# Performance work log

Measured on AMD Instinct MI355X. Metric: run time of the kernel, lower is better.

## Reference

```python
import jax, jax.numpy as jnp
import numpy as np

B, S, D, HEADS, E, HID = 4, 2048, 512, 8, 8, 1365  # HID = int(D*4*2/3) per Expert_alt
CF, THRESH, TOPN = 2.0, 0.2, 2                      # capacity_factor_eval, threshold_eval, top-2
BAL_COEF, Z_COEF = 0.01, 0.001


def setup_inputs():
    key = jax.random.key(0)
    ks = jax.random.split(key, 8)
    f32 = jnp.float32
    return {
        'x': jax.random.normal(ks[0], (B, S, D), f32),
        'Wqkv': jax.random.normal(ks[1], (3 * D, D), f32) * (D ** -0.5),
        'bqkv': jnp.zeros((3 * D,), f32),
        'Wo': jax.random.normal(ks[2], (D, D), f32) * (D ** -0.5),
        'bo': jnp.zeros((D,), f32),
        'Wg': jax.random.normal(ks[3], (D, E), f32) * (D ** -0.5),
        'ln_g': jnp.ones((E, D), f32),
        'ln_b': jnp.zeros((E, D), f32),
        'W1': jax.random.normal(ks[4], (E, D, HID), f32) * (D ** -0.5),
        'b1': jnp.zeros((E, HID), f32),
        'W2': jax.random.normal(ks[5], (E, HID, D), f32) * (HID ** -0.5),
        'b2': jnp.zeros((E, D), f32),
    }


def _moe(x, Wg, ln_g, ln_b, W1, b1, W2, b2):
    # top-2 gated MoE with capacity-factor dispatch, grouped expert FFN, combine
    Bq, Sq, Dq = x.shape
    Eq = Wg.shape[1]
    C = int(CF * Sq * TOPN / Eq)  # expert capacity per batch row
    logits = x @ Wg                              # [B,S,E]
    probs = jax.nn.softmax(logits, -1)
    gvals, gidx = jax.lax.top_k(probs, 2)        # [B,S,2]
    use2 = (gvals[..., 1] > THRESH).astype(x.dtype)
    # priority order: all top-1 assignments first, then top-2
    e_idx = jnp.concatenate([gidx[..., 0], gidx[..., 1]], axis=1)          # [B,2S]
    assigned = jnp.concatenate([jnp.ones((Bq, Sq), x.dtype), use2], axis=1)
    onehot = jax.nn.one_hot(e_idx, Eq, dtype=x.dtype) * assigned[..., None]
    pos = (jnp.cumsum(onehot, axis=1) * onehot).sum(-1) - 1.0              # slot within expert
    keep = ((assigned > 0) & (pos >= 0) & (pos < C)).astype(x.dtype)
    slot = jnp.where(keep > 0, pos, C).astype(jnp.int32)                   # overflow -> slot C (dropped)
    b_idx = jnp.broadcast_to(jnp.arange(Bq)[:, None], (Bq, 2 * Sq))
    x2 = jnp.concatenate([x, x], axis=1) * keep[..., None]
    disp = jnp.zeros((Bq, Eq, C + 1, Dq), x.dtype).at[b_idx, e_idx, slot].add(x2)
    # grouped expert FFN: LayerNorm -> Linear -> LeakyReLU -> Linear
    xe = disp[:, :, :C].transpose(1, 0, 2, 3).reshape(Eq, Bq * C, Dq)
    mu = xe.mean(-1, keepdims=True)
    var = xe.var(-1, keepdims=True)
    xn = (xe - mu) * jax.lax.rsqrt(var + 1e-5) * ln_g[:, None] + ln_b[:, None]
    h = jnp.einsum('etd,edh->eth', xn, W1) + b1[:, None]
    h = jnp.where(h > 0, h, 0.01 * h)  # LeakyReLU
    ye = jnp.einsum('eth,ehd->etd', h, W2) + b2[:, None]
    yb = ye.reshape(Eq, Bq, C, Dq).transpose(1, 0, 2, 3)                   # [B,E,C,D]
    yb = jnp.concatenate([yb, jnp.zeros((Bq, Eq, 1, Dq), x.dtype)], axis=2)
    y_tok = yb[b_idx, e_idx, slot]                                         # [B,2S,D]
    w = jnp.concatenate([gvals[..., 0], gvals[..., 1] * use2], axis=1) * keep
    out = (y_tok * w[..., None]).reshape(Bq, 2, Sq, Dq).sum(1)
    # aux losses
    top1 = jax.nn.one_hot(gidx[..., 0], Eq, dtype=x.dtype)
    density = top1.mean((0, 1))
    proxy = probs.mean((0, 1))
    balance = Eq * jnp.sum(density * proxy)
    zloss = jnp.mean(jax.nn.logsumexp(logits, -1) ** 2)
    total = BAL_COEF * balance + Z_COEF * zloss
    return out, total, balance, zloss


def reference(x, Wqkv, bqkv, Wo, bo, Wg, ln_g, ln_b, W1, b1, W2, b2):
    Bq, Sq, Dq = x.shape
    dh = Dq // HEADS
    qkv = x @ Wqkv.T + bqkv
    q, k, v = jnp.split(qkv, 3, -1)
    rs = lambda t: t.reshape(Bq, Sq, HEADS, dh).transpose(0, 2, 1, 3)
    q, k, v = rs(q), rs(k), rs(v)
    attn = jax.nn.softmax(jnp.einsum('bhqd,bhkd->bhqk', q, k) / np.float32(np.sqrt(dh)), -1)
    o = jnp.einsum('bhqk,bhkd->bhqd', attn, v).transpose(0, 2, 1, 3).reshape(Bq, Sq, Dq)
    o = o @ Wo.T + bo + x  # MHA + residual
    moe_out, total, bal, z = _moe(o, Wg, ln_g, ln_b, W1, b1, W2, b2)
    return moe_out + o, total, bal, z  # SparseMoEBlock residual; dropout is identity (eval)
```

## Files before the change

### kernel.cpp

```cpp
#include <hip/hip_runtime.h>
#include <hip/hip_bf16.h>
#include <math.h>

#define B_    4
#define S_    2048
#define D_    512
#define H_    8
#define DH_   64
#define E_    8
#define HID_  1365
#define HIDP_ 1408
#define CAP_  1024
#define TOK_  (B_*S_)
#define NASS_ (B_*2*S_)
#define RMAX_ (NASS_ + 8*128)
#define NQKU_ 1152
#define C11   (1.0f/2048.0f)
#define C22   (1.0f/(2048.0f*2048.0f))

typedef __attribute__((ext_vector_type(8))) short bf16x8;
typedef __attribute__((ext_vector_type(8))) _Float16 f16x8;
typedef __attribute__((ext_vector_type(2))) __fp16 h16x2;
typedef __attribute__((ext_vector_type(4))) float f32x4;
typedef __hip_bfloat16 bf16;
typedef _Float16 f16;

#define MFMA16(a, b, c) __builtin_amdgcn_mfma_f32_16x16x32_bf16(a, b, c, 0, 0, 0)
#define MFMAH(a, b, c)  __builtin_amdgcn_mfma_f32_16x16x32_f16(a, b, c, 0, 0, 0)

__device__ __forceinline__ void gload16(const void* g, void* l) {
  __builtin_amdgcn_global_load_lds(
      (const __attribute__((address_space(1))) unsigned int*)g,
      (__attribute__((address_space(3))) unsigned int*)l, 16, 0, 0);
}

__device__ __forceinline__ unsigned bf16pk(float a, float b) {
  unsigned ua = __float_as_uint(a); ua = (ua + 0x7FFF + ((ua >> 16) & 1)) >> 16;
  unsigned ub = __float_as_uint(b); ub = (ub + 0x7FFF + ((ub >> 16) & 1)) >> 16;
  return ua | (ub << 16);
}

__device__ __forceinline__ unsigned short h2us(f16 h) {
  return *(unsigned short*)&h;
}

__global__ __launch_bounds__(256) void cvt_bf16(const float* __restrict__ in,
                                                bf16* __restrict__ out, int n) {
  int i = (blockIdx.x * 256 + threadIdx.x) * 4;
  if (i < n) {
    float4 v = *(const float4*)(in + i);
    uint2 pk; pk.x = bf16pk(v.x, v.y); pk.y = bf16pk(v.z, v.w);
    *(uint2*)((unsigned short*)out + i) = pk;
  }
}

__global__ __launch_bounds__(256) void cvt_f16(const float* __restrict__ in,
                                               f16* __restrict__ out, int n) {
  int i = (blockIdx.x * 256 + threadIdx.x) * 4;
  if (i < n) {
    float4 v = *(const float4*)(in + i);
    ushort4 o;
    ((unsigned short*)&o)[0] = h2us((f16)v.x);
    ((unsigned short*)&o)[1] = h2us((f16)v.y);
    ((unsigned short*)&o)[2] = h2us((f16)v.z);
    ((unsigned short*)&o)[3] = h2us((f16)v.w);
    *(ushort4*)((unsigned short*)out + i) = o;
  }
}

__global__ __launch_bounds__(256) void split2h(const float* __restrict__ in,
    unsigned short* __restrict__ ph, unsigned short* __restrict__ pl, int n) {
  int i = (blockIdx.x * 256 + threadIdx.x) * 4;
  if (i >= n) return;
  float4 v = *(const float4*)(in + i);
  float a[4] = {v.x, v.y, v.z, v.w};
  ushort4 hh, ll;
#pragma unroll
  for (int j = 0; j < 4; j++) {
    f16 h = (f16)a[j];
    float r = (a[j] - (float)h) * 2048.f;
    f16 l = (f16)r;
    ((unsigned short*)&hh)[j] = h2us(h);
    ((unsigned short*)&ll)[j] = h2us(l);
  }
  *(ushort4*)(ph + i) = hh;
  *(ushort4*)(pl + i) = ll;
}

__global__ __launch_bounds__(256) void transpose_w1(const float* __restrict__ W1,
                                                    bf16* __restrict__ W1t) {
  __shared__ float t[32][33];
  int e = blockIdx.z;
  int n0 = blockIdx.x * 32, d0 = blockIdx.y * 32;
  int tx = threadIdx.x & 31, ty = threadIdx.x >> 5;
  const float* in = W1 + (size_t)e * D_ * HID_;
  bf16* out = W1t + (size_t)e * HIDP_ * D_;
#pragma unroll
  for (int j = 0; j < 4; j++) {
    int d = d0 + ty + j * 8, n = n0 + tx;
    t[ty + j * 8][tx] = (n < HID_) ? in[(size_t)d * HID_ + n] : 0.f;
  }
  __syncthreads();
#pragma unroll
  for (int j = 0; j < 4; j++) {
    int n = n0 + ty + j * 8, d = d0 + tx;
    out[(size_t)n * D_ + d] = __float2bfloat16(t[tx][ty + j * 8]);
  }
}

__global__ __launch_bounds__(256) void transpose_w2(const float* __restrict__ W2,
                                                    bf16* __restrict__ W2t) {
  __shared__ float t[32][33];
  int e = blockIdx.z;
  int n0 = blockIdx.x * 32, k0 = blockIdx.y * 32;
  int tx = threadIdx.x & 31, ty = threadIdx.x >> 5;
  const float* in = W2 + (size_t)e * HID_ * D_;
  bf16* out = W2t + (size_t)e * D_ * HIDP_;
#pragma unroll
  for (int j = 0; j < 4; j++) {
    int k = k0 + ty + j * 8;
    t[ty + j * 8][tx] = (k < HID_) ? in[(size_t)k * D_ + n0 + tx] : 0.f;
  }
  __syncthreads();
#pragma unroll
  for (int j = 0; j < 4; j++) {
    int n = n0 + ty + j * 8, k = k0 + tx;
    out[(size_t)n * HIDP_ + k] = __float2bfloat16(t[tx][ty + j * 8]);
  }
}

__global__ __launch_bounds__(256) void transpose_v(const unsigned short* __restrict__ vbuf,
                                                   unsigned short* __restrict__ vT) {
  __shared__ unsigned short t[32][33];
  int bh = blockIdx.z;
  int b = bh >> 3, h = bh & 7;
  int s0 = blockIdx.x * 32, d0 = blockIdx.y * 32;
  int tx = threadIdx.x & 31, ty = threadIdx.x >> 5;
  const unsigned short* in = vbuf + (size_t)b * S_ * D_ + h * DH_;
#pragma unroll
  for (int j = 0; j < 4; j++)
    t[ty + j * 8][tx] = in[(size_t)(s0 + ty + j * 8) * D_ + d0 + tx];
  __syncthreads();
  unsigned short* out = vT + (size_t)bh * DH_ * S_;
#pragma unroll
  for (int j = 0; j < 4; j++)
    out[(size_t)(d0 + ty + j * 8) * S_ + s0 + tx] = t[tx][ty + j * 8];
}

__global__ __launch_bounds__(256) void transpose_u(const float* __restrict__ qku,
                                                   f16* __restrict__ U2T) {
  __shared__ float t[64][132];
  int b = blockIdx.y;
  int s0 = blockIdx.x * 64;
  int tid = threadIdx.x;
#pragma unroll
  for (int p = 0; p < 8; p++) {
    int i = tid + p * 256;
    int tok = i >> 5, c4 = i & 31;
    float4 v = *(const float4*)(qku + (size_t)(b * 2048 + s0 + tok) * NQKU_ + 1024 + c4 * 4);
    t[tok][c4 * 4 + 0] = v.x; t[tok][c4 * 4 + 1] = v.y;
    t[tok][c4 * 4 + 2] = v.z; t[tok][c4 * 4 + 3] = v.w;
  }
  __syncthreads();
  int row = tid >> 1, sh = tid & 1;
  int h = row >> 4, rr = row & 15;
  int e = rr & 7;
  bool lo = rr >= 8;
  f16* dst = U2T + ((size_t)((b * 8 + h) * 16 + rr) * 2048 + s0 + sh * 32);
  for (int i = 0; i < 32; i++) {
    float v = t[sh * 32 + i][h * 8 + e];
    f16 hh = (f16)v;
    f16 outv = lo ? (f16)((v - (float)hh) * 2048.f) : hh;
    dst[i] = outv;
  }
}

template <int MODE>
__global__ __launch_bounds__(256) void gemm_mfma(
    const bf16* __restrict__ A, const bf16* __restrict__ Bt,
    const float* __restrict__ bias, const float* __restrict__ resid,
    void* __restrict__ Cout, int N, int K,
    const int* __restrict__ ebase, const int* __restrict__ ecnt) {
  __shared__ bf16 Al[128 * 64];
  __shared__ bf16 Bl[128 * 64];
  int tid = threadIdx.x;
  int w = tid >> 6, lane = tid & 63;
  int lg = lane >> 4, li = lane & 15;
  int e = 0;
  size_t arow0;
  if constexpr (MODE >= 2) {
    e = blockIdx.z;
    int r0 = blockIdx.y * 128;
    if (r0 >= ecnt[e]) return;
    arow0 = (size_t)(ebase[e] + r0);
  } else {
    arow0 = (size_t)blockIdx.y * 128;
  }
  int n0 = blockIdx.x * 128;
  const bf16* Bexp = Bt + (size_t)e * N * K;

  int rowA[4], scA[4];
#pragma unroll
  for (int j = 0; j < 4; j++) {
    int o = w * 4096 + j * 1024 + lane * 16;
    rowA[j] = o >> 7;
    scA[j] = ((o >> 4) & 7) ^ (rowA[j] & 7);
  }
  int wm = w >> 1, wn = w & 1;
  f32x4 acc[4][4] = {};

  for (int k0 = 0; k0 < K; k0 += 64) {
#pragma unroll
    for (int j = 0; j < 4; j++) {
      int o = w * 4096 + j * 1024 + lane * 16;
      gload16(A + (arow0 + rowA[j]) * (size_t)K + k0 + scA[j] * 8, (char*)Al + o);
      gload16(Bexp + (size_t)(n0 + rowA[j]) * K + k0 + scA[j] * 8, (char*)Bl + o);
    }
    __syncthreads();
#pragma unroll
    for (int ks = 0; ks < 2; ks++) {
      bf16x8 af[4], bfr[4];
#pragma unroll
      for (int mi = 0; mi < 4; mi++) {
        int row = wm * 64 + mi * 16 + li;
        int cb = (lg * 16 + ks * 64) ^ ((row & 7) << 4);
        af[mi] = *(const bf16x8*)((char*)Al + row * 128 + cb);
      }
#pragma unroll
      for (int ni = 0; ni < 4; ni++) {
        int row = wn * 64 + ni * 16 + li;
        int cb = (lg * 16 + ks * 64) ^ ((row & 7) << 4);
        bfr[ni] = *(const bf16x8*)((char*)Bl + row * 128 + cb);
      }
#pragma unroll
      for (int mi = 0; mi < 4; mi++)
#pragma unroll
        for (int ni = 0; ni < 4; ni++)
          acc[mi][ni] = MFMA16(af[mi], bfr[ni], acc[mi][ni]);
    }
    __syncthreads();
  }

#pragma unroll
  for (int mi = 0; mi < 4; mi++) {
#pragma unroll
    for (int ni = 0; ni < 4; ni++) {
#pragma unroll
      for (int r = 0; r < 4; r++) {
        size_t m = arow0 + wm * 64 + mi * 16 + lg * 4 + r;
        int c = n0 + wn * 64 + ni * 16 + li;
        float v = acc[mi][ni][r];
        if constexpr (MODE == 1) {
          v += bias[c] + resid[m * (size_t)N + c];
          ((float*)Cout)[m * (size_t)N + c] = v;
        } else if constexpr (MODE == 2) {
          if (c < HID_) {
            v += bias[e * HID_ + c];
            v = (v > 0.f) ? v : 0.01f * v;
            ((bf16*)Cout)[m * (size_t)HIDP_ + c] = __float2bfloat16(v);
          } else {
            ((bf16*)Cout)[m * (size_t)HIDP_ + c] = __float2bfloat16(0.f);
          }
        } else {
          v += bias[e * D_ + c];
          ((bf16*)Cout)[m * (size_t)N + c] = __float2bfloat16(v);
        }
      }
    }
  }
}

__global__ __launch_bounds__(256) void gemm_vf16(
    const f16* __restrict__ A, const f16* __restrict__ Bt,
    const float* __restrict__ bias, f16* __restrict__ Cout, int N, int K) {
  __shared__ f16 Al[128 * 64];
  __shared__ f16 Bl[128 * 64];
  int tid = threadIdx.x;
  int w = tid >> 6, lane = tid & 63;
  int lg = lane >> 4, li = lane & 15;
  size_t arow0 = (size_t)blockIdx.y * 128;
  int n0 = blockIdx.x * 128;

  int rowA[4], scA[4];
#pragma unroll
  for (int j = 0; j < 4; j++) {
    int o = w * 4096 + j * 1024 + lane * 16;
    rowA[j] = o >> 7;
    scA[j] = ((o >> 4) & 7) ^ (rowA[j] & 7);
  }
  int wm = w >> 1, wn = w & 1;
  f32x4 acc[4][4] = {};

  for (int k0 = 0; k0 < K; k0 += 64) {
#pragma unroll
    for (int j = 0; j < 4; j++) {
      int o = w * 4096 + j * 1024 + lane * 16;
      gload16(A + (arow0 + rowA[j]) * (size_t)K + k0 + scA[j] * 8, (char*)Al + o);
      gload16(Bt + (size_t)(n0 + rowA[j]) * K + k0 + scA[j] * 8, (char*)Bl + o);
    }
    __syncthreads();
#pragma unroll
    for (int ks = 0; ks < 2; ks++) {
      f16x8 af[4], bfr[4];
#pragma unroll
      for (int mi = 0; mi < 4; mi++) {
        int row = wm * 64 + mi * 16 + li;
        int cb = (lg * 16 + ks * 64) ^ ((row & 7) << 4);
        af[mi] = *(const f16x8*)((char*)Al + row * 128 + cb);
      }
#pragma unroll
      for (int ni = 0; ni < 4; ni++) {
        int row = wn * 64 + ni * 16 + li;
        int cb = (lg * 16 + ks * 64) ^ ((row & 7) << 4);
        bfr[ni] = *(const f16x8*)((char*)Bl + row * 128 + cb);
      }
#pragma unroll
      for (int mi = 0; mi < 4; mi++)
#pragma unroll
        for (int ni = 0; ni < 4; ni++)
          acc[mi][ni] = MFMAH(af[mi], bfr[ni], acc[mi][ni]);
    }
    __syncthreads();
  }
#pragma unroll
  for (int mi = 0; mi < 4; mi++)
#pragma unroll
    for (int ni = 0; ni < 4; ni++)
#pragma unroll
      for (int r = 0; r < 4; r++) {
        size_t m = arow0 + wm * 64 + mi * 16 + lg * 4 + r;
        int c = n0 + wn * 64 + ni * 16 + li;
        Cout[m * (size_t)N + c] = (f16)(acc[mi][ni][r] + bias[c]);
      }
}

__global__ __launch_bounds__(256) void gemm_split2(
    const f16* __restrict__ Ah, const f16* __restrict__ Als,
    const f16* __restrict__ Bh, const f16* __restrict__ Bls,
    const float* __restrict__ bias, float* __restrict__ C, int N, int K) {
  __shared__ f16 As[2][128 * 64];
  __shared__ f16 Bs[2][128 * 64];
  int tid = threadIdx.x;
  int w = tid >> 6, lane = tid & 63;
  int lg = lane >> 4, li = lane & 15;
  int lin = blockIdx.y * gridDim.x + blockIdx.x;
  int aa = lin / 72, t = lin % 72;
  size_t m0 = (size_t)((t & 7) + 8 * aa) * 128;
  int n0 = (t >> 3) * 128;
  int wm = w >> 1, wn = w & 1;
  f32x4 accA[4][4] = {};
  f32x4 accB[4][4] = {};

  int rowA[4], scA[4];
#pragma unroll
  for (int j = 0; j < 4; j++) {
    int o = w * 4096 + j * 1024 + lane * 16;
    rowA[j] = o >> 7;
    scA[j] = ((o >> 4) & 7) ^ (rowA[j] & 7);
  }

  for (int k0 = 0; k0 < K; k0 += 64) {
#pragma unroll
    for (int j = 0; j < 4; j++) {
      int o = w * 4096 + j * 1024 + lane * 16;
      size_t sa = (m0 + rowA[j]) * (size_t)K + k0 + scA[j] * 8;
      size_t sb = ((size_t)n0 + rowA[j]) * K + k0 + scA[j] * 8;
      gload16(Ah + sa, (char*)As[0] + o);
      gload16(Als + sa, (char*)As[1] + o);
      gload16(Bh + sb, (char*)Bs[0] + o);
      gload16(Bls + sb, (char*)Bs[1] + o);
    }
    __syncthreads();
#pragma unroll
    for (int ks = 0; ks < 2; ks++) {
      f16x8 afh[4], afl[4], bfh[4], bfl[4];
#pragma unroll
      for (int mi = 0; mi < 4; mi++) {
        int row = wm * 64 + mi * 16 + li;
        int cb = (lg * 16 + ks * 64) ^ ((row & 7) << 4);
        afh[mi] = *(const f16x8*)((char*)As[0] + row * 128 + cb);
        afl[mi] = *(const f16x8*)((char*)As[1] + row * 128 + cb);
      }
#pragma unroll
      for (int ni = 0; ni < 4; ni++) {
        int row = wn * 64 + ni * 16 + li;
        int cb = (lg * 16 + ks * 64) ^ ((row & 7) << 4);
        bfh[ni] = *(const f16x8*)((char*)Bs[0] + row * 128 + cb);
        bfl[ni] = *(const f16x8*)((char*)Bs[1] + row * 128 + cb);
      }
#pragma unroll
      for (int mi = 0; mi < 4; mi++)
#pragma unroll
        for (int ni = 0; ni < 4; ni++) {
          accA[mi][ni] = MFMAH(afh[mi], bfh[ni], accA[mi][ni]);
          accB[mi][ni] = MFMAH(afh[mi], bfl[ni], accB[mi][ni]);
          accB[mi][ni] = MFMAH(afl[mi], bfh[ni], accB[mi][ni]);
        }
    }
    __syncthreads();
  }
#pragma unroll
  for (int mi = 0; mi < 4; mi++)
#pragma unroll
    for (int ni = 0; ni < 4; ni++)
#pragma unroll
      for (int r = 0; r < 4; r++) {
        size_t m = m0 + wm * 64 + mi * 16 + lg * 4 + r;
        int c = n0 + wn * 64 + ni * 16 + li;
        C[m * (size_t)N + c] = accA[mi][ni][r] + accB[mi][ni][r] * C11 + bias[c];
      }
}

__global__ __launch_bounds__(256) void ksplit(const float* __restrict__ qku,
    unsigned short* __restrict__ kh, unsigned short* __restrict__ kls) {
  int gid = blockIdx.x * 256 + threadIdx.x;
  int idx4 = gid * 4;
  int t = idx4 >> 9, c = idx4 & 511;
  int h = c >> 6, d = c & 63;
  int b = t >> 11, s = t & 2047;
  float4 v = *(const float4*)(qku + (size_t)t * NQKU_ + 512 + c);
  float a[4] = {v.x, v.y, v.z, v.w};
  ushort4 hh, ll;
#pragma unroll
  for (int j = 0; j < 4; j++) {
    f16 hv = (f16)a[j];
    f16 lv = (f16)((a[j] - (float)hv) * 2048.f);
    ((unsigned short*)&hh)[j] = h2us(hv);
    ((unsigned short*)&ll)[j] = h2us(lv);
  }
  size_t o = (((size_t)(b * 8 + h) * S_ + s) * 64 + d);
  *(ushort4*)(kh + o) = hh;
  *(ushort4*)(kls + o) = ll;
}

__global__ __launch_bounds__(256) void wg2_kernel(const float* __restrict__ Wo,
                                                  const float* __restrict__ Wg,
                                                  float* __restrict__ Wg2) {
  int gid = blockIdx.x * 256 + threadIdx.x;
  int d = gid >> 3, e = gid & 7;
  float acc = 0.f;
  for (int n = 0; n < D_; n++) acc += Wo[(size_t)n * D_ + d] * Wg[n * E_ + e];
  Wg2[d * E_ + e] = acc;
}

__global__ __launch_bounds__(256) void wu_kernel(const float* __restrict__ Wqkv,
    const float* __restrict__ Wg2, const float* __restrict__ bqkv,
    float* __restrict__ Wu, float* __restrict__ bfull) {
  int gid = blockIdx.x * 256 + threadIdx.x;
  int row = gid >> 9, d = gid & 511;
  float acc = 0.f;
  if (row < 64) {
    int h = row >> 3, e = row & 7;
    const float* wv = Wqkv + (size_t)(1024 + h * 64) * 512 + d;
    const float* wg = Wg2 + h * 64 * 8 + e;
    for (int c = 0; c < 64; c++) acc += wv[(size_t)c * 512] * wg[c * 8];
  }
  Wu[gid] = acc;
  if (gid < 1024) bfull[gid] = bqkv[gid];
  if (gid < 128) {
    float bacc = 0.f;
    if (gid < 64) {
      int h = gid >> 3, e = gid & 7;
      for (int c = 0; c < 64; c++)
        bacc += bqkv[1024 + h * 64 + c] * Wg2[(h * 64 + c) * 8 + e];
    }
    bfull[1024 + gid] = bacc;
  }
}

__global__ __launch_bounds__(256) void xwg_kernel(const float* __restrict__ x,
                                                  const float* __restrict__ bo,
                                                  const float* __restrict__ Wg,
                                                  float* __restrict__ logits) {
  int tid = threadIdx.x;
  int tl = tid >> 3, j = tid & 7;
  int t = blockIdx.x * 32 + tl;
  const float* xr = x + (size_t)t * D_;
  float part[8] = {0, 0, 0, 0, 0, 0, 0, 0};
  for (int d = j; d < D_; d += 8) {
    float xv = xr[d] + bo[d];
    const float* wg = Wg + d * E_;
#pragma unroll
    for (int e = 0; e < 8; e++) part[e] += xv * wg[e];
  }
#pragma unroll
  for (int off = 1; off < 8; off <<= 1)
#pragma unroll
    for (int e = 0; e < 8; e++) part[e] += __shfl_xor(part[e], off);
  if (j == 0) {
#pragma unroll
    for (int e = 0; e < 8; e++) logits[(size_t)t * 8 + e] = part[e];
  }
}

__global__ __launch_bounds__(256, 4) void attn_fused(
    const float* __restrict__ qku,
    const f16* __restrict__ kh, const f16* __restrict__ kls,
    const f16* __restrict__ vT, const f16* __restrict__ U2T,
    bf16* __restrict__ attnb, float* __restrict__ part) {
  __shared__ f16 Ks0[64 * 64];
  __shared__ f16 Ks1[64 * 64];
  __shared__ f16 Vtl[64 * 64];
  __shared__ f16 Ut[16 * 64];
  __shared__ f16 Pl[4][16 * 40];
  int bid = blockIdx.x;
  int xcd = bid & 7, idx = bid >> 3;
  int bh = (idx >> 5) * 8 + xcd;
  int qt = idx & 31;
  int b = bh >> 3, h = bh & 7, q0 = qt * 64;
  int tid = threadIdx.x, w = tid >> 6, lane = tid & 63;
  int lg = lane >> 4, qi = lane & 15;
  const float KS = 0.125f * 1.44269504089f;
  const float KS2 = KS * C11;

  const float* qsrc = qku + (size_t)(b * S_ + q0 + w * 16 + qi) * NQKU_ + h * 64 + lg * 8;
  f16x8 qh[2], qls[2];
#pragma unroll
  for (int ks = 0; ks < 2; ks++) {
#pragma unroll
    for (int i = 0; i < 8; i++) {
      float xv = qsrc[ks * 32 + i];
      f16 hh = (f16)xv;
      f16 ll = (f16)((xv - (float)hh) * 2048.f);
      qh[ks][i] = hh;
      qls[ks][i] = ll;
    }
  }

  f32x4 oacc[4] = {};
  f32x4 raccA = {0.f, 0.f, 0.f, 0.f};
  f32x4 raccB = {0.f, 0.f, 0.f, 0.f};
  float mrun = -1e30f, lrun = 0.f;
  const f16* Vbase = vT + (size_t)bh * DH_ * S_;
  char* pw = (char*)&Pl[w][0];

  for (int kt = 0; kt < S_ / 64; kt++) {
#pragma unroll
    for (int j = 0; j < 2; j++) {
      int o = w * 2048 + j * 1024 + lane * 16;
      int row = o >> 7;
      int sc = ((o >> 4) & 7) ^ (row & 7);
      size_t srcK = ((size_t)bh * S_ + kt * 64 + row) * 64 + sc * 8;
      gload16(kh + srcK, (char*)Ks0 + o);
      gload16(kls + srcK, (char*)Ks1 + o);
      gload16(Vbase + (size_t)row * S_ + kt * 64 + sc * 8, (char*)Vtl + o);
    }
    if (w < 2) {
      int o = w * 1024 + lane * 16;
      int rowu = o >> 7;
      int scu = ((o >> 4) & 7) ^ (rowu & 7);
      gload16(U2T + ((size_t)(bh * 16 + rowu) * 2048 + kt * 64 + scu * 8),
              (char*)Ut + o);
    }
    __syncthreads();

    f32x4 sA[4];
    float tmax = -1e30f;
#pragma unroll
    for (int nb = 0; nb < 4; nb++) {
      f32x4 a = {0.f, 0.f, 0.f, 0.f};
      f32x4 bq = {0.f, 0.f, 0.f, 0.f};
      int row = nb * 16 + qi;
#pragma unroll
      for (int ks = 0; ks < 2; ks++) {
        int cb = (lg * 16 + ks * 64) ^ ((row & 7) << 4);
        f16x8 k0 = *(const f16x8*)((char*)Ks0 + row * 128 + cb);
        f16x8 k1 = *(const f16x8*)((char*)Ks1 + row * 128 + cb);
        a = MFMAH(k0, qh[ks], a);
        bq = MFMAH(k0, qls[ks], bq);
        bq = MFMAH(k1, qh[ks], bq);
      }
#pragma unroll
      for (int r = 0; r < 4; r++) {
        float v = a[r] * KS + bq[r] * KS2;
        sA[nb][r] = v;
        tmax = fmaxf(tmax, v);
      }
    }
    tmax = fmaxf(tmax, __shfl_xor(tmax, 16));
    tmax = fmaxf(tmax, __shfl_xor(tmax, 32));
    float fsc = 1.f;
    if (!__all(tmax <= mrun + 8.f)) {
      float mnew = fmaxf(mrun, tmax);
      fsc = exp2f(mrun - mnew);
      mrun = mnew;
#pragma unroll
      for (int r = 0; r < 4; r++) { raccA[r] *= fsc; raccB[r] *= fsc; }
#pragma unroll
      for (int db = 0; db < 4; db++)
#pragma unroll
        for (int r = 0; r < 4; r++) oacc[db][r] *= fsc;
    }
    float psum = 0.f;
#pragma unroll
    for (int nb = 0; nb < 4; nb++)
#pragma unroll
      for (int r = 0; r < 4; r++) {
        float pv = exp2f(sA[nb][r] - mrun);
        sA[nb][r] = pv;
        psum += pv;
      }
    psum += __shfl_xor(psum, 16);
    psum += __shfl_xor(psum, 32);
    lrun = lrun * fsc + psum;

#pragma unroll
    for (int c = 0; c < 2; c++) {
#pragma unroll
      for (int nbL = 0; nbL < 2; nbL++)
#pragma unroll
        for (int rp = 0; rp < 2; rp++) {
          int nb = c * 2 + nbL;
          float p0 = sA[nb][rp * 2], p1 = sA[nb][rp * 2 + 1];
          h16x2 hp = __builtin_amdgcn_cvt_pkrtz(p0, p1);
          int keyl = 4 * lg + 2 * rp + 16 * nbL;
          *(unsigned*)(pw + qi * 80 + keyl * 2) = *(unsigned*)&hp;
        }
      f16x8 pf = *(const f16x8*)(pw + qi * 80 + lg * 16);
#pragma unroll
      for (int db = 0; db < 4; db++) {
        int row = db * 16 + qi;
        int cb = (lg * 16 + c * 64) ^ ((row & 7) << 4);
        f16x8 vf = *(const f16x8*)((char*)Vtl + row * 128 + cb);
        oacc[db] = MFMAH(vf, pf, oacc[db]);
      }
      int ua = qi * 128 + ((c * 64 + lg * 16) ^ ((qi & 7) << 4));
      f16x8 uf = *(const f16x8*)((char*)Ut + ua);
      raccA = MFMAH(uf, pf, raccA);
#pragma unroll
      for (int nbL = 0; nbL < 2; nbL++)
#pragma unroll
        for (int rp = 0; rp < 2; rp++) {
          int nb = c * 2 + nbL;
          float p0 = sA[nb][rp * 2], p1 = sA[nb][rp * 2 + 1];
          h16x2 hp = __builtin_amdgcn_cvt_pkrtz(p0, p1);
          float b0 = (float)hp[0], b1 = (float)hp[1];
          h16x2 lp = __builtin_amdgcn_cvt_pkrtz((p0 - b0) * 2048.f, (p1 - b1) * 2048.f);
          int keyl = 4 * lg + 2 * rp + 16 * nbL;
          *(unsigned*)(pw + qi * 80 + keyl * 2) = *(unsigned*)&lp;
        }
      f16x8 pfl = *(const f16x8*)(pw + qi * 80 + lg * 16);
      raccB = MFMAH(uf, pfl, raccB);
    }
    __syncthreads();
  }

  float inv = 1.f / lrun;
  f32x4 pA, pB;
#pragma unroll
  for (int r = 0; r < 4; r++) {
    pA[r] = __shfl_xor(raccA[r], 32);
    pB[r] = __shfl_xor(raccB[r], 32);
  }
  if (lg < 2) {
    float* dst = part + ((size_t)bh * S_ + q0 + w * 16 + qi) * 8 + lg * 4;
#pragma unroll
    for (int r = 0; r < 4; r++)
      dst[r] = (raccA[r] + C11 * (pA[r] + raccB[r]) + C22 * pB[r]) * inv;
  }
  char* ow = (char*)Ks0 + w * 2048;
#pragma unroll
  for (int db = 0; db < 4; db++)
#pragma unroll
    for (int rp = 0; rp < 2; rp++) {
      int d = db * 16 + lg * 4 + rp * 2;
      unsigned pk = bf16pk(oacc[db][rp * 2] * inv, oacc[db][rp * 2 + 1] * inv);
      int addr = (qi * 128 + d * 2) ^ ((qi & 7) << 4);
      *(unsigned*)(ow + addr) = pk;
    }
#pragma unroll
  for (int j = 0; j < 2; j++) {
    int o = j * 1024 + lane * 16;
    int q = o >> 7;
    int c16 = (o >> 4) & 7;
    int sc = c16 ^ (q & 7);
    bf16x8 vv = *(const bf16x8*)(ow + q * 128 + sc * 16);
    *(bf16x8*)(attnb + ((size_t)(b * S_ + q0 + w * 16 + q)) * D_ + h * DH_ + c16 * 8) = vv;
  }
}

__global__ __launch_bounds__(256) void reduce_gate(
    const float* __restrict__ xwg, const float* __restrict__ part,
    int* __restrict__ e1a, int* __restrict__ e2a,
    float* __restrict__ g1a, float* __restrict__ g2a, int* __restrict__ use2a,
    float* __restrict__ dacc) {
  int t = blockIdx.x * 256 + threadIdx.x;
  int b = t >> 11, s = t & 2047;
  float lg[8];
#pragma unroll
  for (int e = 0; e < 8; e++) lg[e] = xwg[(size_t)t * 8 + e];
  for (int h = 0; h < 8; h++) {
    const float* pp = part + ((size_t)(b * 8 + h) * S_ + s) * 8;
#pragma unroll
    for (int e = 0; e < 8; e++) lg[e] += pp[e];
  }
  float mx = lg[0];
#pragma unroll
  for (int e = 1; e < 8; e++) mx = fmaxf(mx, lg[e]);
  float p[8], se = 0.f;
#pragma unroll
  for (int e = 0; e < 8; e++) { p[e] = expf(lg[e] - mx); se += p[e]; }
  float inv = 1.f / se;
#pragma unroll
  for (int e = 0; e < 8; e++) p[e] *= inv;
  float lse = logf(se) + mx;
  int a1 = 0; float m1 = p[0];
#pragma unroll
  for (int e = 1; e < 8; e++) if (p[e] > m1) { m1 = p[e]; a1 = e; }
  int a2 = -1; float m2 = -1.f;
#pragma unroll
  for (int e = 0; e < 8; e++) if (e != a1 && p[e] > m2) { m2 = p[e]; a2 = e; }
  e1a[t] = a1; e2a[t] = a2; g1a[t] = m1; g2a[t] = m2;
  use2a[t] = (m2 > 0.2f) ? 1 : 0;
  float z = lse * lse;
  float pr[8];
#pragma unroll
  for (int e = 0; e < 8; e++) pr[e] = p[e];
#pragma unroll
  for (int off = 1; off < 64; off <<= 1) {
#pragma unroll
    for (int e = 0; e < 8; e++) pr[e] += __shfl_xor(pr[e], off);
    z += __shfl_xor(z, off);
  }
  float dcnt[8];
#pragma unroll
  for (int e = 0; e < 8; e++) dcnt[e] = (float)__popcll(__ballot(a1 == e));
  if ((threadIdx.x & 63) == 0) {
#pragma unroll
    for (int e = 0; e < 8; e++) {
      atomicAdd(&dacc[e], dcnt[e]);
      atomicAdd(&dacc[8 + e], pr[e]);
    }
    atomicAdd(&dacc[16], z);
  }
}

__global__ __launch_bounds__(512) void scan_kernel(
    const int* __restrict__ e1a, const int* __restrict__ e2a,
    const int* __restrict__ use2a,
    int* __restrict__ posArr, int* __restrict__ kept_be) {
  __shared__ int wcnt[8][8];
  int b = blockIdx.x;
  int w = threadIdx.x >> 6, lane = threadIdx.x & 63;
  unsigned long long below = (1ull << lane) - 1ull;
  int cnt[8] = {0, 0, 0, 0, 0, 0, 0, 0};
  int ev[8], av[8];
#pragma unroll
  for (int it = 0; it < 8; it++) {
    int i = w * 512 + it * 64 + lane;
    int s = i & (S_ - 1);
    int t = b * S_ + s;
    int e, a;
    if (i < S_) { e = e1a[t]; a = 1; }
    else        { e = e2a[t]; a = use2a[t]; }
    ev[it] = e; av[it] = a;
#pragma unroll
    for (int ee = 0; ee < 8; ee++)
      cnt[ee] += __popcll(__ballot(a && (e == ee)));
  }
  if (lane == 0)
#pragma unroll
    for (int ee = 0; ee < 8; ee++) wcnt[w][ee] = cnt[ee];
  __syncthreads();
  int run[8];
#pragma unroll
  for (int ee = 0; ee < 8; ee++) {
    int sB = 0;
    for (int ww = 0; ww < w; ww++) sB += wcnt[ww][ee];
    run[ee] = sB;
  }
#pragma unroll
  for (int it = 0; it < 8; it++) {
    int i = w * 512 + it * 64 + lane;
    int e = ev[it], a = av[it];
    int pos = -1;
#pragma unroll
    for (int ee = 0; ee < 8; ee++) {
      unsigned long long mask = __ballot(a && (e == ee));
      if (a && e == ee) pos = run[ee] + __popcll(mask & below);
      run[ee] += __popcll(mask);
    }
    posArr[b * (2 * S_) + i] = (a && pos < CAP_) ? pos : -1;
  }
  if (w == 7 && lane == 0)
#pragma unroll
    for (int ee = 0; ee < 8; ee++) kept_be[b * 8 + ee] = min(run[ee], CAP_);
}

__global__ void finalize_meta(const int* __restrict__ kept_be,
                              int* __restrict__ ebase, int* __restrict__ bbase,
                              int* __restrict__ ecnt,
                              const float* __restrict__ dacc, float* __restrict__ outs) {
  if (threadIdx.x == 0 && blockIdx.x == 0) {
    int base = 0;
    for (int e = 0; e < 8; e++) {
      int tot = 0;
      for (int b = 0; b < 4; b++) { bbase[b * 8 + e] = tot; tot += kept_be[b * 8 + e]; }
      ecnt[e] = tot;
      ebase[e] = base;
      base += (tot + 127) & ~127;
    }
    float bal = 0.f;
    for (int e = 0; e < 8; e++) bal += (dacc[e] / (float)TOK_) * (dacc[8 + e] / (float)TOK_);
    bal *= (float)E_;
    float z = dacc[16] / (float)TOK_;
    outs[0] = 0.01f * bal + 0.001f * z;
    outs[1] = bal;
    outs[2] = z;
  }
}

__global__ __launch_bounds__(256) void scatter_kernel(
    const int* __restrict__ posArr, const int* __restrict__ e1a, const int* __restrict__ e2a,
    const float* __restrict__ g1a, const float* __restrict__ g2a,
    const int* __restrict__ ebase, const int* __restrict__ bbase,
    int* __restrict__ rowtok, int* __restrict__ rowexp,
    int* __restrict__ tokidx, float* __restrict__ tokw) {
  int gi = blockIdx.x * 256 + threadIdx.x;
  int b = gi >> 12, i = gi & 4095;
  int k = i >> 11, s = i & (S_ - 1);
  int t = b * S_ + s;
  int pos = posArr[gi];
  int idx = -1; float w = 0.f;
  if (pos >= 0) {
    int e = k ? e2a[t] : e1a[t];
    idx = ebase[e] + bbase[b * 8 + e] + pos;
    rowtok[idx] = t;
    rowexp[idx] = e;
    w = k ? g2a[t] : g1a[t];
  }
  tokidx[k * TOK_ + t] = idx;
  tokw[k * TOK_ + t] = w;
}

__global__ __launch_bounds__(256) void ln_kernel(
    const float* __restrict__ o2, const int* __restrict__ rowtok,
    const int* __restrict__ rowexp, const float* __restrict__ ln_g,
    const float* __restrict__ ln_b, bf16* __restrict__ xn) {
  int row = blockIdx.x * 4 + (threadIdx.x >> 6);
  int lane = threadIdx.x & 63;
  int tok = rowtok[row];
  if (tok < 0) return;
  int e = rowexp[row];
  const float* xr = o2 + (size_t)tok * D_;
  float v[8], sum = 0.f, sq = 0.f;
#pragma unroll
  for (int j = 0; j < 8; j++) { v[j] = xr[lane * 8 + j]; sum += v[j]; sq += v[j] * v[j]; }
#pragma unroll
  for (int off = 1; off < 64; off <<= 1) { sum += __shfl_xor(sum, off); sq += __shfl_xor(sq, off); }
  float mu = sum / (float)D_;
  float var = sq / (float)D_ - mu * mu;
  float inv = rsqrtf(var + 1e-5f);
  bf16* xo = xn + (size_t)row * D_;
#pragma unroll
  for (int j = 0; j < 8; j++) {
    int d = lane * 8 + j;
    xo[d] = __float2bfloat16((v[j] - mu) * inv * ln_g[e * D_ + d] + ln_b[e * D_ + d]);
  }
}

__global__ __launch_bounds__(256) void combine_kernel(
    const float* __restrict__ o2, const bf16* __restrict__ y,
    const int* __restrict__ tokidx, const float* __restrict__ tokw,
    float* __restrict__ out) {
  size_t gi = (size_t)blockIdx.x * 256 + threadIdx.x;
  int t = (int)(gi >> 9);
  int d = (int)(gi & (D_ - 1));
  float v = o2[gi];
  int i1 = tokidx[t], i2 = tokidx[TOK_ + t];
  if (i1 >= 0) v += tokw[t] * __bfloat162float(y[(size_t)i1 * D_ + d]);
  if (i2 >= 0) v += tokw[TOK_ + t] * __bfloat162float(y[(size_t)i2 * D_ + d]);
  out[gi] = v;
}

extern "C" void kernel_launch(void* const* d_in, const int* in_sizes, int n_in,
                              void* d_out, int out_size, void* d_ws, size_t ws_size,
                              hipStream_t stream) {
  const float* x    = (const float*)d_in[0];
  const float* Wqkv = (const float*)d_in[1];
  const float* bqkv = (const float*)d_in[2];
  const float* Wo   = (const float*)d_in[3];
  const float* bo   = (const float*)d_in[4];
  const float* Wg   = (const float*)d_in[5];
  const float* ln_g = (const float*)d_in[6];
  const float* ln_b = (const float*)d_in[7];
  const float* W1   = (const float*)d_in[8];
  const float* b1   = (const float*)d_in[9];
  const float* W2   = (const float*)d_in[10];
  const float* b2   = (const float*)d_in[11];
  float* out = (float*)d_out;

  char* ws = (char*)d_ws;
  size_t off = 0;
  auto alloc = [&](size_t bytes) -> void* {
    void* p = ws + off;
    off = (off + bytes + 255) & ~(size_t)255;
    return p;
  };
  float* qku32 = (float*)alloc((size_t)TOK_ * NQKU_ * 4);
  f16*  vbuf   = (f16*)alloc((size_t)TOK_ * D_ * 2);
  f16*  vT     = (f16*)alloc((size_t)B_ * H_ * DH_ * S_ * 2);
  bf16* attnb  = (bf16*)alloc((size_t)TOK_ * D_ * 2);
  float* o2    = (float*)alloc((size_t)TOK_ * D_ * 4);
  f16*  xh     = (f16*)alloc((size_t)TOK_ * D_ * 2);
  f16*  xls    = (f16*)alloc((size_t)TOK_ * D_ * 2);
  f16*  Wqh    = (f16*)alloc((size_t)NQKU_ * D_ * 2);
  f16*  Wqls   = (f16*)alloc((size_t)NQKU_ * D_ * 2);
  f16*  Wvh    = (f16*)alloc((size_t)D_ * D_ * 2);
  bf16* Wob    = (bf16*)alloc((size_t)D_ * D_ * 2);
  bf16* W1t    = (bf16*)alloc((size_t)E_ * HIDP_ * D_ * 2);
  bf16* W2t    = (bf16*)alloc((size_t)E_ * D_ * HIDP_ * 2);
  bf16* xn     = (bf16*)alloc((size_t)RMAX_ * D_ * 2);
  bf16* hbuf   = (bf16*)alloc((size_t)RMAX_ * HIDP_ * 2);
  bf16* ybuf   = (bf16*)alloc((size_t)RMAX_ * D_ * 2);
  float* Wg2   = (float*)alloc(D_ * E_ * 4);
  float* Wu    = (float*)alloc((size_t)128 * D_ * 4);
  float* bfull = (float*)alloc(NQKU_ * 4);
  f16*  U2T    = (f16*)alloc((size_t)32 * 16 * 2048 * 2);
  float* logits= (float*)alloc((size_t)TOK_ * 8 * 4);
  float* part  = (float*)alloc((size_t)B_ * H_ * S_ * 8 * 4);
  int*   e1a   = (int*)alloc(TOK_ * 4);
  int*   e2a   = (int*)alloc(TOK_ * 4);
  int*   use2a = (int*)alloc(TOK_ * 4);
  float* g1a   = (float*)alloc(TOK_ * 4);
  float* g2a   = (float*)alloc(TOK_ * 4);
  int*   posArr  = (int*)alloc(NASS_ * 4);
  int*   kept_be = (int*)alloc(32 * 4);
  int*   ebase   = (int*)alloc(8 * 4);
  int*   bbase   = (int*)alloc(32 * 4);
  int*   ecnt    = (int*)alloc(8 * 4);
  int*   rowtok  = (int*)alloc(RMAX_ * 4);
  int*   rowexp  = (int*)alloc(RMAX_ * 4);
  int*   tokidx  = (int*)alloc(NASS_ * 4);
  float* tokw    = (float*)alloc(NASS_ * 4);
  float* dacc    = (float*)alloc(32 * 4);
  f16* kh  = xh;
  f16* kls = xls;

  hipMemsetAsync(dacc, 0, 32 * 4, stream);
  hipMemsetAsync(rowtok, 0xFF, RMAX_ * 4, stream);

  split2h<<<TOK_ * D_ / 4 / 256, 256, 0, stream>>>(x, (unsigned short*)xh,
                                                   (unsigned short*)xls, TOK_ * D_);
  split2h<<<1024 * D_ / 4 / 256, 256, 0, stream>>>(Wqkv, (unsigned short*)Wqh,
                                                   (unsigned short*)Wqls, 1024 * D_);
  cvt_f16<<<D_ * D_ / 4 / 256, 256, 0, stream>>>(Wqkv + (size_t)1024 * D_, Wvh, D_ * D_);
  cvt_bf16<<<D_ * D_ / 4 / 256, 256, 0, stream>>>(Wo, Wob, D_ * D_);
  transpose_w1<<<dim3(44, 16, 8), 256, 0, stream>>>(W1, W1t);
  transpose_w2<<<dim3(16, 44, 8), 256, 0, stream>>>(W2, W2t);
  wg2_kernel<<<16, 256, 0, stream>>>(Wo, Wg, Wg2);
  wu_kernel<<<256, 256, 0, stream>>>(Wqkv, Wg2, bqkv, Wu, bfull);
  split2h<<<128 * D_ / 4 / 256, 256, 0, stream>>>(Wu,
      (unsigned short*)(Wqh + (size_t)1024 * D_),
      (unsigned short*)(Wqls + (size_t)1024 * D_), 128 * D_);

  gemm_split2<<<dim3(9, 64), 256, 0, stream>>>(xh, xls, Wqh, Wqls,
                                               bfull, qku32, NQKU_, D_);
  gemm_vf16<<<dim3(4, 64), 256, 0, stream>>>(xh, Wvh, bqkv + 1024, vbuf, D_, D_);
  ksplit<<<TOK_ * 512 / 4 / 256, 256, 0, stream>>>(qku32, (unsigned short*)kh,
                                                   (unsigned short*)kls);
  transpose_u<<<dim3(32, 4), 256, 0, stream>>>(qku32, U2T);
  xwg_kernel<<<TOK_ / 32, 256, 0, stream>>>(x, bo, Wg, logits);
  transpose_v<<<dim3(64, 2, 32), 256, 0, stream>>>((const unsigned short*)vbuf,
                                                   (unsigned short*)vT);

  attn_fused<<<dim3(1024), 256, 0, stream>>>(qku32, kh, kls, vT, U2T,
                                             attnb, part);
  gemm_mfma<1><<<dim3(4, 64), 256, 0, stream>>>(attnb, Wob, bo, x, o2,
                                                D_, D_, nullptr, nullptr);
  reduce_gate<<<TOK_ / 256, 256, 0, stream>>>(logits, part, e1a, e2a, g1a, g2a,
                                              use2a, dacc);
  scan_kernel<<<B_, 512, 0, stream>>>(e1a, e2a, use2a, posArr, kept_be);
  finalize_meta<<<1, 64, 0, stream>>>(kept_be, ebase, bbase, ecnt, dacc,
                                      out + (size_t)TOK_ * D_);
  scatter_kernel<<<NASS_ / 256, 256, 0, stream>>>(posArr, e1a, e2a, g1a, g2a,
                                                  ebase, bbase, rowtok, rowexp,
                                                  tokidx, tokw);
  ln_kernel<<<RMAX_ / 4, 256, 0, stream>>>(o2, rowtok, rowexp, ln_g, ln_b, xn);
  gemm_mfma<2><<<dim3(HIDP_ / 128, 32, E_), 256, 0, stream>>>(xn, W1t, b1, nullptr, hbuf,
                                                              HIDP_, D_, ebase, ecnt);
  gemm_mfma<3><<<dim3(D_ / 128, 32, E_), 256, 0, stream>>>(hbuf, W2t, b2, nullptr, ybuf,
                                                           D_, HIDP_, ebase, ecnt);
  combine_kernel<<<(TOK_ * D_) / 256, 256, 0, stream>>>(o2, ybuf, tokidx, tokw, out);
}
```

Baseline: 473.4 us.

## Merge independent prep, projection and gating kernels into fewer multi-role launches

```diff
diff --git a/kernel.cpp b/kernel.cpp
--- a/kernel.cpp
+++ b/kernel.cpp
@@ -44,33 +44,11 @@
   return *(unsigned short*)&h;
 }
 
-__global__ __launch_bounds__(256) void cvt_bf16(const float* __restrict__ in,
-                                                bf16* __restrict__ out, int n) {
-  int i = (blockIdx.x * 256 + threadIdx.x) * 4;
-  if (i < n) {
-    float4 v = *(const float4*)(in + i);
-    uint2 pk; pk.x = bf16pk(v.x, v.y); pk.y = bf16pk(v.z, v.w);
-    *(uint2*)((unsigned short*)out + i) = pk;
-  }
-}
-
-__global__ __launch_bounds__(256) void cvt_f16(const float* __restrict__ in,
-                                               f16* __restrict__ out, int n) {
-  int i = (blockIdx.x * 256 + threadIdx.x) * 4;
-  if (i < n) {
-    float4 v = *(const float4*)(in + i);
-    ushort4 o;
-    ((unsigned short*)&o)[0] = h2us((f16)v.x);
-    ((unsigned short*)&o)[1] = h2us((f16)v.y);
-    ((unsigned short*)&o)[2] = h2us((f16)v.z);
-    ((unsigned short*)&o)[3] = h2us((f16)v.w);
-    *(ushort4*)((unsigned short*)out + i) = o;
-  }
-}
-
-__global__ __launch_bounds__(256) void split2h(const float* __restrict__ in,
-    unsigned short* __restrict__ ph, unsigned short* __restrict__ pl, int n) {
-  int i = (blockIdx.x * 256 + threadIdx.x) * 4;
+
+__device__ __forceinline__ void dev_split2h(const float* __restrict__ in,
+    unsigned short* __restrict__ ph, unsigned short* __restrict__ pl,
+    int n, int vb) {
+  int i = (vb * 256 + threadIdx.x) * 4;
   if (i >= n) return;
   float4 v = *(const float4*)(in + i);
   float a[4] = {v.x, v.y, v.z, v.w};
@@ -87,79 +65,111 @@
   *(ushort4*)(pl + i) = ll;
 }
 
-__global__ __launch_bounds__(256) void transpose_w1(const float* __restrict__ W1,
-                                                    bf16* __restrict__ W1t) {
-  __shared__ float t[32][33];
-  int e = blockIdx.z;
-  int n0 = blockIdx.x * 32, d0 = blockIdx.y * 32;
+__device__ __forceinline__ void dev_cvt_f16(const float* __restrict__ in,
+                                            f16* __restrict__ out, int n, int vb) {
+  int i = (vb * 256 + threadIdx.x) * 4;
+  if (i >= n) return;
+  float4 v = *(const float4*)(in + i);
+  ushort4 o;
+  ((unsigned short*)&o)[0] = h2us((f16)v.x);
+  ((unsigned short*)&o)[1] = h2us((f16)v.y);
+  ((unsigned short*)&o)[2] = h2us((f16)v.z);
+  ((unsigned short*)&o)[3] = h2us((f16)v.w);
+  *(ushort4*)((unsigned short*)out + i) = o;
+}
+
+__device__ __forceinline__ void dev_cvt_bf16(const float* __restrict__ in,
+                                             bf16* __restrict__ out, int n, int vb) {
+  int i = (vb * 256 + threadIdx.x) * 4;
+  if (i >= n) return;
+  float4 v = *(const float4*)(in + i);
+  uint2 pk; pk.x = bf16pk(v.x, v.y); pk.y = bf16pk(v.z, v.w);
+  *(uint2*)((unsigned short*)out + i) = pk;
+}
+
+__device__ __forceinline__ void dev_transpose_w1(const float* __restrict__ W1,
+    bf16* __restrict__ W1t, int vb, float* sm) {
+  int xg = vb % 44, yg = (vb / 44) % 16, e = vb / 704;
+  int n0 = xg * 32, d0 = yg * 32;
   int tx = threadIdx.x & 31, ty = threadIdx.x >> 5;
   const float* in = W1 + (size_t)e * D_ * HID_;
   bf16* out = W1t + (size_t)e * HIDP_ * D_;
 #pragma unroll
   for (int j = 0; j < 4; j++) {
     int d = d0 + ty + j * 8, n = n0 + tx;
-    t[ty + j * 8][tx] = (n < HID_) ? in[(size_t)d * HID_ + n] : 0.f;
+    sm[(ty + j * 8) * 33 + tx] = (n < HID_) ? in[(size_t)d * HID_ + n] : 0.f;
   }
   __syncthreads();
 #pragma unroll
   for (int j = 0; j < 4; j++) {
     int n = n0 + ty + j * 8, d = d0 + tx;
-    out[(size_t)n * D_ + d] = __float2bfloat16(t[tx][ty + j * 8]);
-  }
-}
-
-__global__ __launch_bounds__(256) void transpose_w2(const float* __restrict__ W2,
-                                                    bf16* __restrict__ W2t) {
-  __shared__ float t[32][33];
-  int e = blockIdx.z;
-  int n0 = blockIdx.x * 32, k0 = blockIdx.y * 32;
+    out[(size_t)n * D_ + d] = __float2bfloat16(sm[tx * 33 + ty + j * 8]);
+  }
+}
+
+__device__ __forceinline__ void dev_transpose_w2(const float* __restrict__ W2,
+    bf16* __restrict__ W2t, int vb, float* sm) {
+  int xg = vb % 16, yg = (vb / 16) % 44, e = vb / 704;
+  int n0 = xg * 32, k0 = yg * 32;
   int tx = threadIdx.x & 31, ty = threadIdx.x >> 5;
   const float* in = W2 + (size_t)e * HID_ * D_;
   bf16* out = W2t + (size_t)e * D_ * HIDP_;
 #pragma unroll
   for (int j = 0; j < 4; j++) {
     int k = k0 + ty + j * 8;
-    t[ty + j * 8][tx] = (k < HID_) ? in[(size_t)k * D_ + n0 + tx] : 0.f;
+    sm[(ty + j * 8) * 33 + tx] = (k < HID_) ? in[(size_t)k * D_ + n0 + tx] : 0.f;
   }
   __syncthreads();
 #pragma unroll
   for (int j = 0; j < 4; j++) {
     int n = n0 + ty + j * 8, k = k0 + tx;
-    out[(size_t)n * HIDP_ + k] = __float2bfloat16(t[tx][ty + j * 8]);
-  }
-}
-
-__global__ __launch_bounds__(256) void transpose_v(const unsigned short* __restrict__ vbuf,
-                                                   unsigned short* __restrict__ vT) {
-  __shared__ unsigned short t[32][33];
-  int bh = blockIdx.z;
-  int b = bh >> 3, h = bh & 7;
-  int s0 = blockIdx.x * 32, d0 = blockIdx.y * 32;
-  int tx = threadIdx.x & 31, ty = threadIdx.x >> 5;
-  const unsigned short* in = vbuf + (size_t)b * S_ * D_ + h * DH_;
-#pragma unroll
-  for (int j = 0; j < 4; j++)
-    t[ty + j * 8][tx] = in[(size_t)(s0 + ty + j * 8) * D_ + d0 + tx];
-  __syncthreads();
-  unsigned short* out = vT + (size_t)bh * DH_ * S_;
-#pragma unroll
-  for (int j = 0; j < 4; j++)
-    out[(size_t)(d0 + ty + j * 8) * S_ + s0 + tx] = t[tx][ty + j * 8];
-}
-
-__global__ __launch_bounds__(256) void transpose_u(const float* __restrict__ qku,
-                                                   f16* __restrict__ U2T) {
-  __shared__ float t[64][132];
-  int b = blockIdx.y;
-  int s0 = blockIdx.x * 64;
+    out[(size_t)n * HIDP_ + k] = __float2bfloat16(sm[tx * 33 + ty + j * 8]);
+  }
+}
+
+__device__ __forceinline__ void dev_wg2(const float* __restrict__ Wo,
+    const float* __restrict__ Wg, float* __restrict__ Wg2, int vb) {
+  int gid = vb * 256 + threadIdx.x;
+  int d = gid >> 3, e = gid & 7;
+  float acc = 0.f;
+  for (int n = 0; n < D_; n++) acc += Wo[(size_t)n * D_ + d] * Wg[n * E_ + e];
+  Wg2[d * E_ + e] = acc;
+}
+
+__device__ __forceinline__ void dev_ksplit(const float* __restrict__ qku,
+    unsigned short* __restrict__ kh, unsigned short* __restrict__ kls, int vb) {
+  int gid = vb * 256 + threadIdx.x;
+  int idx4 = gid * 4;
+  int t = idx4 >> 9, c = idx4 & 511;
+  int h = c >> 6, d = c & 63;
+  int b = t >> 11, s = t & 2047;
+  float4 v = *(const float4*)(qku + (size_t)t * NQKU_ + 512 + c);
+  float a[4] = {v.x, v.y, v.z, v.w};
+  ushort4 hh, ll;
+#pragma unroll
+  for (int j = 0; j < 4; j++) {
+    f16 hv = (f16)a[j];
+    f16 lv = (f16)((a[j] - (float)hv) * 2048.f);
+    ((unsigned short*)&hh)[j] = h2us(hv);
+    ((unsigned short*)&ll)[j] = h2us(lv);
+  }
+  size_t o = (((size_t)(b * 8 + h) * S_ + s) * 64 + d);
+  *(ushort4*)(kh + o) = hh;
+  *(ushort4*)(kls + o) = ll;
+}
+
+__device__ __forceinline__ void dev_transpose_u(const float* __restrict__ qku,
+    f16* __restrict__ U2T, int bx, int by, float* sm) {
+  int b = by;
+  int s0 = bx * 64;
   int tid = threadIdx.x;
 #pragma unroll
   for (int p = 0; p < 8; p++) {
     int i = tid + p * 256;
     int tok = i >> 5, c4 = i & 31;
     float4 v = *(const float4*)(qku + (size_t)(b * 2048 + s0 + tok) * NQKU_ + 1024 + c4 * 4);
-    t[tok][c4 * 4 + 0] = v.x; t[tok][c4 * 4 + 1] = v.y;
-    t[tok][c4 * 4 + 2] = v.z; t[tok][c4 * 4 + 3] = v.w;
+    sm[tok * 132 + c4 * 4 + 0] = v.x; sm[tok * 132 + c4 * 4 + 1] = v.y;
+    sm[tok * 132 + c4 * 4 + 2] = v.z; sm[tok * 132 + c4 * 4 + 3] = v.w;
   }
   __syncthreads();
   int row = tid >> 1, sh = tid & 1;
@@ -168,11 +178,287 @@
   bool lo = rr >= 8;
   f16* dst = U2T + ((size_t)((b * 8 + h) * 16 + rr) * 2048 + s0 + sh * 32);
   for (int i = 0; i < 32; i++) {
-    float v = t[sh * 32 + i][h * 8 + e];
+    float v = sm[(sh * 32 + i) * 132 + h * 8 + e];
     f16 hh = (f16)v;
     f16 outv = lo ? (f16)((v - (float)hh) * 2048.f) : hh;
     dst[i] = outv;
   }
+}
+
+__device__ __forceinline__ void dev_xwg(const float* __restrict__ x,
+    const float* __restrict__ bo, const float* __restrict__ Wg,
+    float* __restrict__ logits, int vb) {
+  int tid = threadIdx.x;
+  int tl = tid >> 3, j = tid & 7;
+  int t = vb * 32 + tl;
+  const float* xr = x + (size_t)t * D_;
+  float part[8] = {0, 0, 0, 0, 0, 0, 0, 0};
+  for (int d = j; d < D_; d += 8) {
+    float xv = xr[d] + bo[d];
+    const float* wg = Wg + d * E_;
+#pragma unroll
+    for (int e = 0; e < 8; e++) part[e] += xv * wg[e];
+  }
+#pragma unroll
+  for (int off = 1; off < 8; off <<= 1)
+#pragma unroll
+    for (int e = 0; e < 8; e++) part[e] += __shfl_xor(part[e], off);
+  if (j == 0) {
+#pragma unroll
+    for (int e = 0; e < 8; e++) logits[(size_t)t * 8 + e] = part[e];
+  }
+}
+
+__device__ __forceinline__ void dev_transpose_v(
+    const unsigned short* __restrict__ vbuf, unsigned short* __restrict__ vT,
+    int vb, unsigned short* sm) {
+  int xg = vb & 63, yg = (vb >> 6) & 1, bh = vb >> 7;
+  int b = bh >> 3, h = bh & 7;
+  int s0 = xg * 32, d0 = yg * 32;
+  int tx = threadIdx.x & 31, ty = threadIdx.x >> 5;
+  const unsigned short* in = vbuf + (size_t)b * S_ * D_ + h * DH_;
+#pragma unroll
+  for (int j = 0; j < 4; j++)
+    sm[(ty + j * 8) * 33 + tx] = in[(size_t)(s0 + ty + j * 8) * D_ + d0 + tx];
+  __syncthreads();
+  unsigned short* out = vT + (size_t)bh * DH_ * S_;
+#pragma unroll
+  for (int j = 0; j < 4; j++)
+    out[(size_t)(d0 + ty + j * 8) * S_ + s0 + tx] = sm[tx * 33 + ty + j * 8];
+}
+
+__global__ __launch_bounds__(256) void prep_a(
+    const float* __restrict__ x, const float* __restrict__ Wqkv,
+    const float* __restrict__ Wo, const float* __restrict__ W1,
+    const float* __restrict__ W2, const float* __restrict__ Wg,
+    unsigned short* __restrict__ xh, unsigned short* __restrict__ xls,
+    unsigned short* __restrict__ Wqh, unsigned short* __restrict__ Wqls,
+    f16* __restrict__ Wvh, bf16* __restrict__ Wob,
+    bf16* __restrict__ W1t, bf16* __restrict__ W2t, float* __restrict__ Wg2,
+    int* __restrict__ rowtok, float* __restrict__ dacc) {
+  __shared__ float smem[32 * 33];
+  int bid = blockIdx.x;
+  if (bid < 68) { rowtok[bid * 256 + threadIdx.x] = -1; return; }
+  bid -= 68;
+  if (bid < 1) { if (threadIdx.x < 32) dacc[threadIdx.x] = 0.f; return; }
+  bid -= 1;
+  if (bid < 4096) { dev_split2h(x, xh, xls, TOK_ * D_, bid); return; }
+  bid -= 4096;
+  if (bid < 512) { dev_split2h(Wqkv, Wqh, Wqls, 1024 * D_, bid); return; }
+  bid -= 512;
+  if (bid < 256) { dev_cvt_f16(Wqkv + (size_t)1024 * D_, Wvh, D_ * D_, bid); return; }
+  bid -= 256;
+  if (bid < 256) { dev_cvt_bf16(Wo, Wob, D_ * D_, bid); return; }
+  bid -= 256;
+  if (bid < 5632) { dev_transpose_w1(W1, W1t, bid, smem); return; }
+  bid -= 5632;
+  if (bid < 5632) { dev_transpose_w2(W2, W2t, bid, smem); return; }
+  bid -= 5632;
+  dev_wg2(Wo, Wg, Wg2, bid);
+}
+
+__global__ __launch_bounds__(256) void wu_kernel2(const float* __restrict__ Wqkv,
+    const float* __restrict__ Wg2, const float* __restrict__ bqkv,
+    unsigned short* __restrict__ WqhT, unsigned short* __restrict__ WqlsT,
+    float* __restrict__ bfull) {
+  int gid = blockIdx.x * 256 + threadIdx.x;
+  int row = gid >> 9, d = gid & 511;
+  float acc = 0.f;
+  if (row < 64) {
+    int h = row >> 3, e = row & 7;
+    const float* wv = Wqkv + (size_t)(1024 + h * 64) * 512 + d;
+    const float* wg = Wg2 + h * 64 * 8 + e;
+    for (int c = 0; c < 64; c++) acc += wv[(size_t)c * 512] * wg[c * 8];
+  }
+  f16 hv = (f16)acc;
+  f16 lv = (f16)((acc - (float)hv) * 2048.f);
+  WqhT[gid] = h2us(hv);
+  WqlsT[gid] = h2us(lv);
+  if (gid < 1024) bfull[gid] = bqkv[gid];
+  if (gid < 128) {
+    float bacc = 0.f;
+    if (gid < 64) {
+      int h = gid >> 3, e = gid & 7;
+      for (int c = 0; c < 64; c++)
+        bacc += bqkv[1024 + h * 64 + c] * Wg2[(h * 64 + c) * 8 + e];
+    }
+    bfull[1024 + gid] = bacc;
+  }
+}
+
+__device__ void dev_gemm_split2(
+    const f16* __restrict__ Ah, const f16* __restrict__ Als,
+    const f16* __restrict__ Bh, const f16* __restrict__ Bls,
+    const float* __restrict__ bias, float* __restrict__ C, int N, int K,
+    int lin, f16* sh) {
+  f16* As0 = sh;
+  f16* As1 = sh + 8192;
+  f16* Bs0 = sh + 16384;
+  f16* Bs1 = sh + 24576;
+  int tid = threadIdx.x;
+  int w = tid >> 6, lane = tid & 63;
+  int lg = lane >> 4, li = lane & 15;
+  int aa = lin / 72, t = lin % 72;
+  size_t m0 = (size_t)((t & 7) + 8 * aa) * 128;
+  int n0 = (t >> 3) * 128;
+  int wm = w >> 1, wn = w & 1;
+  f32x4 accA[4][4] = {};
+  f32x4 accB[4][4] = {};
+
+  int rowA[4], scA[4];
+#pragma unroll
+  for (int j = 0; j < 4; j++) {
+    int o = w * 4096 + j * 1024 + lane * 16;
+    rowA[j] = o >> 7;
+    scA[j] = ((o >> 4) & 7) ^ (rowA[j] & 7);
+  }
+
+  for (int k0 = 0; k0 < K; k0 += 64) {
+#pragma unroll
+    for (int j = 0; j < 4; j++) {
+      int o = w * 4096 + j * 1024 + lane * 16;
+      size_t sa = (m0 + rowA[j]) * (size_t)K + k0 + scA[j] * 8;
+      size_t sb = ((size_t)n0 + rowA[j]) * K + k0 + scA[j] * 8;
+      gload16(Ah + sa, (char*)As0 + o);
+      gload16(Als + sa, (char*)As1 + o);
+      gload16(Bh + sb, (char*)Bs0 + o);
+      gload16(Bls + sb, (char*)Bs1 + o);
+    }
+    __syncthreads();
+#pragma unroll
+    for (int ks = 0; ks < 2; ks++) {
+      f16x8 afh[4], afl[4], bfh[4], bfl[4];
+#pragma unroll
+      for (int mi = 0; mi < 4; mi++) {
+        int row = wm * 64 + mi * 16 + li;
+        int cb = (lg * 16 + ks * 64) ^ ((row & 7) << 4);
+        afh[mi] = *(const f16x8*)((char*)As0 + row * 128 + cb);
+        afl[mi] = *(const f16x8*)((char*)As1 + row * 128 + cb);
+      }
+#pragma unroll
+      for (int ni = 0; ni < 4; ni++) {
+        int row = wn * 64 + ni * 16 + li;
+        int cb = (lg * 16 + ks * 64) ^ ((row & 7) << 4);
+        bfh[ni] = *(const f16x8*)((char*)Bs0 + row * 128 + cb);
+        bfl[ni] = *(const f16x8*)((char*)Bs1 + row * 128 + cb);
+      }
+#pragma unroll
+      for (int mi = 0; mi < 4; mi++)
+#pragma unroll
+        for (int ni = 0; ni < 4; ni++) {
+          accA[mi][ni] = MFMAH(afh[mi], bfh[ni], accA[mi][ni]);
+          accB[mi][ni] = MFMAH(afh[mi], bfl[ni], accB[mi][ni]);
+          accB[mi][ni] = MFMAH(afl[mi], bfh[ni], accB[mi][ni]);
+        }
+    }
+    __syncthreads();
+  }
+#pragma unroll
+  for (int mi = 0; mi < 4; mi++)
+#pragma unroll
+    for (int ni = 0; ni < 4; ni++)
+#pragma unroll
+      for (int r = 0; r < 4; r++) {
+        size_t m = m0 + wm * 64 + mi * 16 + lg * 4 + r;
+        int c = n0 + wn * 64 + ni * 16 + li;
+        C[m * (size_t)N + c] = accA[mi][ni][r] + accB[mi][ni][r] * C11 + bias[c];
+      }
+}
+
+__device__ void dev_gemm_vf16(
+    const f16* __restrict__ A, const f16* __restrict__ Bt,
+    const float* __restrict__ bias, f16* __restrict__ Cout, int N, int K,
+    int vb, f16* sh) {
+  f16* Al = sh;
+  f16* Bl = sh + 8192;
+  int tid = threadIdx.x;
+  int w = tid >> 6, lane = tid & 63;
+  int lg = lane >> 4, li = lane & 15;
+  size_t arow0 = (size_t)(vb >> 2) * 128;
+  int n0 = (vb & 3) * 128;
+
+  int rowA[4], scA[4];
+#pragma unroll
+  for (int j = 0; j < 4; j++) {
+    int o = w * 4096 + j * 1024 + lane * 16;
+    rowA[j] = o >> 7;
+    scA[j] = ((o >> 4) & 7) ^ (rowA[j] & 7);
+  }
+  int wm = w >> 1, wn = w & 1;
+  f32x4 acc[4][4] = {};
+
+  for (int k0 = 0; k0 < K; k0 += 64) {
+#pragma unroll
+    for (int j = 0; j < 4; j++) {
+      int o = w * 4096 + j * 1024 + lane * 16;
+      gload16(A + (arow0 + rowA[j]) * (size_t)K + k0 + scA[j] * 8, (char*)Al + o);
+      gload16(Bt + (size_t)(n0 + rowA[j]) * K + k0 + scA[j] * 8, (char*)Bl + o);
+    }
+    __syncthreads();
+#pragma unroll
+    for (int ks = 0; ks < 2; ks++) {
+      f16x8 af[4], bfr[4];
+#pragma unroll
+      for (int mi = 0; mi < 4; mi++) {
+        int row = wm * 64 + mi * 16 + li;
+        int cb = (lg * 16 + ks * 64) ^ ((row & 7) << 4);
+        af[mi] = *(const f16x8*)((char*)Al + row * 128 + cb);
+      }
+#pragma unroll
+      for (int ni = 0; ni < 4; ni++) {
+        int row = wn * 64 + ni * 16 + li;
+        int cb = (lg * 16 + ks * 64) ^ ((row & 7) << 4);
+        bfr[ni] = *(const f16x8*)((char*)Bl + row * 128 + cb);
+      }
+#pragma unroll
+      for (int mi = 0; mi < 4; mi++)
+#pragma unroll
+        for (int ni = 0; ni < 4; ni++)
+          acc[mi][ni] = MFMAH(af[mi], bfr[ni], acc[mi][ni]);
+    }
+    __syncthreads();
+  }
+#pragma unroll
+  for (int mi = 0; mi < 4; mi++)
+#pragma unroll
+    for (int ni = 0; ni < 4; ni++)
+#pragma unroll
+      for (int r = 0; r < 4; r++) {
+        size_t m = arow0 + wm * 64 + mi * 16 + lg * 4 + r;
+        int c = n0 + wn * 64 + ni * 16 + li;
+        Cout[m * (size_t)N + c] = (f16)(acc[mi][ni][r] + bias[c]);
+      }
+}
+
+__global__ __launch_bounds__(256) void gemm_qv(
+    const f16* __restrict__ Ah, const f16* __restrict__ Als,
+    const f16* __restrict__ Bh, const f16* __restrict__ Bls,
+    const float* __restrict__ bfull, float* __restrict__ qku32,
+    const f16* __restrict__ Wvh, const float* __restrict__ bv,
+    f16* __restrict__ vbuf) {
+  __shared__ f16 sh[4 * 128 * 64];
+  int bid = blockIdx.x;
+  if (bid < 576)
+    dev_gemm_split2(Ah, Als, Bh, Bls, bfull, qku32, NQKU_, D_, bid, sh);
+  else
+    dev_gemm_vf16(Ah, Wvh, bv, vbuf, D_, D_, bid - 576, sh);
+}
+
+__global__ __launch_bounds__(256) void prep_e(
+    const float* __restrict__ qku, unsigned short* __restrict__ kh,
+    unsigned short* __restrict__ kls, f16* __restrict__ U2T,
+    const float* __restrict__ x, const float* __restrict__ bo,
+    const float* __restrict__ Wg, float* __restrict__ logits,
+    const unsigned short* __restrict__ vbuf, unsigned short* __restrict__ vT) {
+  __shared__ float smem[64 * 132];
+  int bid = blockIdx.x;
+  if (bid < 4096) { dev_ksplit(qku, kh, kls, bid); return; }
+  bid -= 4096;
+  if (bid < 128) { dev_transpose_u(qku, U2T, bid & 31, bid >> 5, smem); return; }
+  bid -= 128;
+  if (bid < 256) { dev_xwg(x, bo, Wg, logits, bid); return; }
+  bid -= 256;
+  dev_transpose_v(vbuf, vT, bid, (unsigned short*)smem);
 }
 
 template <int MODE>
@@ -250,10 +536,7 @@
         size_t m = arow0 + wm * 64 + mi * 16 + lg * 4 + r;
         int c = n0 + wn * 64 + ni * 16 + li;
         float v = acc[mi][ni][r];
-        if constexpr (MODE == 1) {
-          v += bias[c] + resid[m * (size_t)N + c];
-          ((float*)Cout)[m * (size_t)N + c] = v;
-        } else if constexpr (MODE == 2) {
+        if constexpr (MODE == 2) {
           if (c < HID_) {
             v += bias[e * HID_ + c];
             v = (v > 0.f) ? v : 0.01f * v;
@@ -270,16 +553,18 @@
   }
 }
 
-__global__ __launch_bounds__(256) void gemm_vf16(
-    const f16* __restrict__ A, const f16* __restrict__ Bt,
-    const float* __restrict__ bias, f16* __restrict__ Cout, int N, int K) {
-  __shared__ f16 Al[128 * 64];
-  __shared__ f16 Bl[128 * 64];
+__device__ void dev_gemm_wo(
+    const bf16* __restrict__ A, const bf16* __restrict__ Bt,
+    const float* __restrict__ bias, const float* __restrict__ resid,
+    float* __restrict__ Cout, int vb, bf16* sh) {
+  bf16* Al = sh;
+  bf16* Bl = sh + 8192;
+  const int N = D_, K = D_;
   int tid = threadIdx.x;
   int w = tid >> 6, lane = tid & 63;
   int lg = lane >> 4, li = lane & 15;
-  size_t arow0 = (size_t)blockIdx.y * 128;
-  int n0 = blockIdx.x * 128;
+  size_t arow0 = (size_t)(vb >> 2) * 128;
+  int n0 = (vb & 3) * 128;
 
   int rowA[4], scA[4];
 #pragma unroll
@@ -301,24 +586,24 @@
     __syncthreads();
 #pragma unroll
     for (int ks = 0; ks < 2; ks++) {
-      f16x8 af[4], bfr[4];
+      bf16x8 af[4], bfr[4];
 #pragma unroll
       for (int mi = 0; mi < 4; mi++) {
         int row = wm * 64 + mi * 16 + li;
         int cb = (lg * 16 + ks * 64) ^ ((row & 7) << 4);
-        af[mi] = *(const f16x8*)((char*)Al + row * 128 + cb);
+        af[mi] = *(const bf16x8*)((char*)Al + row * 128 + cb);
       }
 #pragma unroll
       for (int ni = 0; ni < 4; ni++) {
         int row = wn * 64 + ni * 16 + li;
         int cb = (lg * 16 + ks * 64) ^ ((row & 7) << 4);
-        bfr[ni] = *(const f16x8*)((char*)Bl + row * 128 + cb);
+        bfr[ni] = *(const bf16x8*)((char*)Bl + row * 128 + cb);
       }
 #pragma unroll
       for (int mi = 0; mi < 4; mi++)
 #pragma unroll
         for (int ni = 0; ni < 4; ni++)
-          acc[mi][ni] = MFMAH(af[mi], bfr[ni], acc[mi][ni]);
+          acc[mi][ni] = MFMA16(af[mi], bfr[ni], acc[mi][ni]);
     }
     __syncthreads();
   }
@@ -330,167 +615,78 @@
       for (int r = 0; r < 4; r++) {
         size_t m = arow0 + wm * 64 + mi * 16 + lg * 4 + r;
         int c = n0 + wn * 64 + ni * 16 + li;
-        Cout[m * (size_t)N + c] = (f16)(acc[mi][ni][r] + bias[c]);
-      }
-}
-
-__global__ __launch_bounds__(256) void gemm_split2(
-    const f16* __restrict__ Ah, const f16* __restrict__ Als,
-    const f16* __restrict__ Bh, const f16* __restrict__ Bls,
-    const float* __restrict__ bias, float* __restrict__ C, int N, int K) {
-  __shared__ f16 As[2][128 * 64];
-  __shared__ f16 Bs[2][128 * 64];
-  int tid = threadIdx.x;
-  int w = tid >> 6, lane = tid & 63;
-  int lg = lane >> 4, li = lane & 15;
-  int lin = blockIdx.y * gridDim.x + blockIdx.x;
-  int aa = lin / 72, t = lin % 72;
-  size_t m0 = (size_t)((t & 7) + 8 * aa) * 128;
-  int n0 = (t >> 3) * 128;
-  int wm = w >> 1, wn = w & 1;
-  f32x4 accA[4][4] = {};
-  f32x4 accB[4][4] = {};
-
-  int rowA[4], scA[4];
-#pragma unroll
-  for (int j = 0; j < 4; j++) {
-    int o = w * 4096 + j * 1024 + lane * 16;
-    rowA[j] = o >> 7;
-    scA[j] = ((o >> 4) & 7) ^ (rowA[j] & 7);
-  }
-
-  for (int k0 = 0; k0 < K; k0 += 64) {
-#pragma unroll
-    for (int j = 0; j < 4; j++) {
-      int o = w * 4096 + j * 1024 + lane * 16;
-      size_t sa = (m0 + rowA[j]) * (size_t)K + k0 + scA[j] * 8;
-      size_t sb = ((size_t)n0 + rowA[j]) * K + k0 + scA[j] * 8;
-      gload16(Ah + sa, (char*)As[0] + o);
-      gload16(Als + sa, (char*)As[1] + o);
-      gload16(Bh + sb, (char*)Bs[0] + o);
-      gload16(Bls + sb, (char*)Bs[1] + o);
-    }
-    __syncthreads();
-#pragma unroll
-    for (int ks = 0; ks < 2; ks++) {
-      f16x8 afh[4], afl[4], bfh[4], bfl[4];
-#pragma unroll
-      for (int mi = 0; mi < 4; mi++) {
-        int row = wm * 64 + mi * 16 + li;
-        int cb = (lg * 16 + ks * 64) ^ ((row & 7) << 4);
-        afh[mi] = *(const f16x8*)((char*)As[0] + row * 128 + cb);
-        afl[mi] = *(const f16x8*)((char*)As[1] + row * 128 + cb);
-      }
-#pragma unroll
-      for (int ni = 0; ni < 4; ni++) {
-        int row = wn * 64 + ni * 16 + li;
-        int cb = (lg * 16 + ks * 64) ^ ((row & 7) << 4);
-        bfh[ni] = *(const f16x8*)((char*)Bs[0] + row * 128 + cb);
-        bfl[ni] = *(const f16x8*)((char*)Bs[1] + row * 128 + cb);
-      }
-#pragma unroll
-      for (int mi = 0; mi < 4; mi++)
-#pragma unroll
-        for (int ni = 0; ni < 4; ni++) {
-          accA[mi][ni] = MFMAH(afh[mi], bfh[ni], accA[mi][ni]);
-          accB[mi][ni] = MFMAH(afh[mi], bfl[ni], accB[mi][ni]);
-          accB[mi][ni] = MFMAH(afl[mi], bfh[ni], accB[mi][ni]);
-        }
-    }
-    __syncthreads();
-  }
-#pragma unroll
-  for (int mi = 0; mi < 4; mi++)
-#pragma unroll
-    for (int ni = 0; ni < 4; ni++)
-#pragma unroll
-      for (int r = 0; r < 4; r++) {
-        size_t m = m0 + wm * 64 + mi * 16 + lg * 4 + r;
-        int c = n0 + wn * 64 + ni * 16 + li;
-        C[m * (size_t)N + c] = accA[mi][ni][r] + accB[mi][ni][r] * C11 + bias[c];
-      }
-}
-
-__global__ __launch_bounds__(256) void ksplit(const float* __restrict__ qku,
-    unsigned short* __restrict__ kh, unsigned short* __restrict__ kls) {
-  int gid = blockIdx.x * 256 + threadIdx.x;
-  int idx4 = gid * 4;
-  int t = idx4 >> 9, c = idx4 & 511;
-  int h = c >> 6, d = c & 63;
+        Cout[m * (size_t)N + c] = acc[mi][ni][r] + bias[c] + resid[m * (size_t)N + c];
+      }
+}
+
+__device__ void dev_reduce_gate(
+    const float* __restrict__ xwg, const float* __restrict__ part,
+    int* __restrict__ e1a, int* __restrict__ e2a,
+    float* __restrict__ g1a, float* __restrict__ g2a, int* __restrict__ use2a,
+    float* __restrict__ dacc, int vb) {
+  int t = vb * 256 + threadIdx.x;
   int b = t >> 11, s = t & 2047;
-  float4 v = *(const float4*)(qku + (size_t)t * NQKU_ + 512 + c);
-  float a[4] = {v.x, v.y, v.z, v.w};
-  ushort4 hh, ll;
-#pragma unroll
-  for (int j = 0; j < 4; j++) {
-    f16 hv = (f16)a[j];
-    f16 lv = (f16)((a[j] - (float)hv) * 2048.f);
-    ((unsigned short*)&hh)[j] = h2us(hv);
-    ((unsigned short*)&ll)[j] = h2us(lv);
-  }
-  size_t o = (((size_t)(b * 8 + h) * S_ + s) * 64 + d);
-  *(ushort4*)(kh + o) = hh;
-  *(ushort4*)(kls + o) = ll;
-}
-
-__global__ __launch_bounds__(256) void wg2_kernel(const float* __restrict__ Wo,
-                                                  const float* __restrict__ Wg,
-                                                  float* __restrict__ Wg2) {
-  int gid = blockIdx.x * 256 + threadIdx.x;
-  int d = gid >> 3, e = gid & 7;
-  float acc = 0.f;
-  for (int n = 0; n < D_; n++) acc += Wo[(size_t)n * D_ + d] * Wg[n * E_ + e];
-  Wg2[d * E_ + e] = acc;
-}
-
-__global__ __launch_bounds__(256) void wu_kernel(const float* __restrict__ Wqkv,
-    const float* __restrict__ Wg2, const float* __restrict__ bqkv,
-    float* __restrict__ Wu, float* __restrict__ bfull) {
-  int gid = blockIdx.x * 256 + threadIdx.x;
-  int row = gid >> 9, d = gid & 511;
-  float acc = 0.f;
-  if (row < 64) {
-    int h = row >> 3, e = row & 7;
-    const float* wv = Wqkv + (size_t)(1024 + h * 64) * 512 + d;
-    const float* wg = Wg2 + h * 64 * 8 + e;
-    for (int c = 0; c < 64; c++) acc += wv[(size_t)c * 512] * wg[c * 8];
-  }
-  Wu[gid] = acc;
-  if (gid < 1024) bfull[gid] = bqkv[gid];
-  if (gid < 128) {
-    float bacc = 0.f;
-    if (gid < 64) {
-      int h = gid >> 3, e = gid & 7;
-      for (int c = 0; c < 64; c++)
-        bacc += bqkv[1024 + h * 64 + c] * Wg2[(h * 64 + c) * 8 + e];
-    }
-    bfull[1024 + gid] = bacc;
-  }
-}
-
-__global__ __launch_bounds__(256) void xwg_kernel(const float* __restrict__ x,
-                                                  const float* __restrict__ bo,
-                                                  const float* __restrict__ Wg,
-                                                  float* __restrict__ logits) {
-  int tid = threadIdx.x;
-  int tl = tid >> 3, j = tid & 7;
-  int t = blockIdx.x * 32 + tl;
-  const float* xr = x + (size_t)t * D_;
-  float part[8] = {0, 0, 0, 0, 0, 0, 0, 0};
-  for (int d = j; d < D_; d += 8) {
-    float xv = xr[d] + bo[d];
-    const float* wg = Wg + d * E_;
-#pragma unroll
-    for (int e = 0; e < 8; e++) part[e] += xv * wg[e];
-  }
-#pragma unroll
-  for (int off = 1; off < 8; off <<= 1)
-#pragma unroll
-    for (int e = 0; e < 8; e++) part[e] += __shfl_xor(part[e], off);
-  if (j == 0) {
-#pragma unroll
-    for (int e = 0; e < 8; e++) logits[(size_t)t * 8 + e] = part[e];
-  }
+  float lg[8];
+#pragma unroll
+  for (int e = 0; e < 8; e++) lg[e] = xwg[(size_t)t * 8 + e];
+  for (int h = 0; h < 8; h++) {
+    const float* pp = part + ((size_t)(b * 8 + h) * S_ + s) * 8;
+#pragma unroll
+    for (int e = 0; e < 8; e++) lg[e] += pp[e];
+  }
+  float mx = lg[0];
+#pragma unroll
+  for (int e = 1; e < 8; e++) mx = fmaxf(mx, lg[e]);
+  float p[8], se = 0.f;
+#pragma unroll
+  for (int e = 0; e < 8; e++) { p[e] = expf(lg[e] - mx); se += p[e]; }
+  float inv = 1.f / se;
+#pragma unroll
+  for (int e = 0; e < 8; e++) p[e] *= inv;
+  float lse = logf(se) + mx;
+  int a1 = 0; float m1 = p[0];
+#pragma unroll
+  for (int e = 1; e < 8; e++) if (p[e] > m1) { m1 = p[e]; a1 = e; }
+  int a2 = -1; float m2 = -1.f;
+#pragma unroll
+  for (int e = 0; e < 8; e++) if (e != a1 && p[e] > m2) { m2 = p[e]; a2 = e; }
+  e1a[t] = a1; e2a[t] = a2; g1a[t] = m1; g2a[t] = m2;
+  use2a[t] = (m2 > 0.2f) ? 1 : 0;
+  float z = lse * lse;
+  float pr[8];
+#pragma unroll
+  for (int e = 0; e < 8; e++) pr[e] = p[e];
+#pragma unroll
+  for (int off = 1; off < 64; off <<= 1) {
+#pragma unroll
+    for (int e = 0; e < 8; e++) pr[e] += __shfl_xor(pr[e], off);
+    z += __shfl_xor(z, off);
+  }
+  float dcnt[8];
+#pragma unroll
+  for (int e = 0; e < 8; e++) dcnt[e] = (float)__popcll(__ballot(a1 == e));
+  if ((threadIdx.x & 63) == 0) {
+#pragma unroll
+    for (int e = 0; e < 8; e++) {
+      atomicAdd(&dacc[e], dcnt[e]);
+      atomicAdd(&dacc[8 + e], pr[e]);
+    }
+    atomicAdd(&dacc[16], z);
+  }
+}
+
+__global__ __launch_bounds__(256) void wo_rg(
+    const bf16* __restrict__ attnb, const bf16* __restrict__ Wob,
+    const float* __restrict__ bo, const float* __restrict__ x,
+    float* __restrict__ o2,
+    const float* __restrict__ xwg, const float* __restrict__ part,
+    int* __restrict__ e1a, int* __restrict__ e2a,
+    float* __restrict__ g1a, float* __restrict__ g2a, int* __restrict__ use2a,
+    float* __restrict__ dacc) {
+  __shared__ bf16 sh[2 * 128 * 64];
+  int bid = blockIdx.x;
+  if (bid < 256) dev_gemm_wo(attnb, Wob, bo, x, o2, bid, sh);
+  else dev_reduce_gate(xwg, part, e1a, e2a, g1a, g2a, use2a, dacc, bid - 256);
 }
 
 __global__ __launch_bounds__(256, 4) void attn_fused(
@@ -676,62 +872,6 @@
     int sc = c16 ^ (q & 7);
     bf16x8 vv = *(const bf16x8*)(ow + q * 128 + sc * 16);
     *(bf16x8*)(attnb + ((size_t)(b * S_ + q0 + w * 16 + q)) * D_ + h * DH_ + c16 * 8) = vv;
-  }
-}
-
-__global__ __launch_bounds__(256) void reduce_gate(
-    const float* __restrict__ xwg, const float* __restrict__ part,
-    int* __restrict__ e1a, int* __restrict__ e2a,
-    float* __restrict__ g1a, float* __restrict__ g2a, int* __restrict__ use2a,
-    float* __restrict__ dacc) {
-  int t = blockIdx.x * 256 + threadIdx.x;
-  int b = t >> 11, s = t & 2047;
-  float lg[8];
-#pragma unroll
-  for (int e = 0; e < 8; e++) lg[e] = xwg[(size_t)t * 8 + e];
-  for (int h = 0; h < 8; h++) {
-    const float* pp = part + ((size_t)(b * 8 + h) * S_ + s) * 8;
-#pragma unroll
-    for (int e = 0; e < 8; e++) lg[e] += pp[e];
-  }
-  float mx = lg[0];
-#pragma unroll
-  for (int e = 1; e < 8; e++) mx = fmaxf(mx, lg[e]);
-  float p[8], se = 0.f;
-#pragma unroll
-  for (int e = 0; e < 8; e++) { p[e] = expf(lg[e] - mx); se += p[e]; }
-  float inv = 1.f / se;
-#pragma unroll
-  for (int e = 0; e < 8; e++) p[e] *= inv;
-  float lse = logf(se) + mx;
-  int a1 = 0; float m1 = p[0];
-#pragma unroll
-  for (int e = 1; e < 8; e++) if (p[e] > m1) { m1 = p[e]; a1 = e; }
-  int a2 = -1; float m2 = -1.f;
-#pragma unroll
-  for (int e = 0; e < 8; e++) if (e != a1 && p[e] > m2) { m2 = p[e]; a2 = e; }
-  e1a[t] = a1; e2a[t] = a2; g1a[t] = m1; g2a[t] = m2;
-  use2a[t] = (m2 > 0.2f) ? 1 : 0;
-  float z = lse * lse;
-  float pr[8];
-#pragma unroll
-  for (int e = 0; e < 8; e++) pr[e] = p[e];
-#pragma unroll
-  for (int off = 1; off < 64; off <<= 1) {
-#pragma unroll
-    for (int e = 0; e < 8; e++) pr[e] += __shfl_xor(pr[e], off);
-    z += __shfl_xor(z, off);
-  }
-  float dcnt[8];
-#pragma unroll
-  for (int e = 0; e < 8; e++) dcnt[e] = (float)__popcll(__ballot(a1 == e));
-  if ((threadIdx.x & 63) == 0) {
-#pragma unroll
-    for (int e = 0; e < 8; e++) {
-      atomicAdd(&dacc[e], dcnt[e]);
-      atomicAdd(&dacc[8 + e], pr[e]);
-    }
-    atomicAdd(&dacc[16], z);
   }
 }
 
@@ -914,7 +1054,6 @@
   bf16* hbuf   = (bf16*)alloc((size_t)RMAX_ * HIDP_ * 2);
   bf16* ybuf   = (bf16*)alloc((size_t)RMAX_ * D_ * 2);
   float* Wg2   = (float*)alloc(D_ * E_ * 4);
-  float* Wu    = (float*)alloc((size_t)128 * D_ * 4);
   float* bfull = (float*)alloc(NQKU_ * 4);
   f16*  U2T    = (f16*)alloc((size_t)32 * 16 * 2048 * 2);
   float* logits= (float*)alloc((size_t)TOK_ * 8 * 4);
@@ -937,39 +1076,23 @@
   f16* kh  = xh;
   f16* kls = xls;
 
-  hipMemsetAsync(dacc, 0, 32 * 4, stream);
-  hipMemsetAsync(rowtok, 0xFF, RMAX_ * 4, stream);
-
-  split2h<<<TOK_ * D_ / 4 / 256, 256, 0, stream>>>(x, (unsigned short*)xh,
-                                                   (unsigned short*)xls, TOK_ * D_);
-  split2h<<<1024 * D_ / 4 / 256, 256, 0, stream>>>(Wqkv, (unsigned short*)Wqh,
-                                                   (unsigned short*)Wqls, 1024 * D_);
-  cvt_f16<<<D_ * D_ / 4 / 256, 256, 0, stream>>>(Wqkv + (size_t)1024 * D_, Wvh, D_ * D_);
-  cvt_bf16<<<D_ * D_ / 4 / 256, 256, 0, stream>>>(Wo, Wob, D_ * D_);
-  transpose_w1<<<dim3(44, 16, 8), 256, 0, stream>>>(W1, W1t);
-  transpose_w2<<<dim3(16, 44, 8), 256, 0, stream>>>(W2, W2t);
-  wg2_kernel<<<16, 256, 0, stream>>>(Wo, Wg, Wg2);
-  wu_kernel<<<256, 256, 0, stream>>>(Wqkv, Wg2, bqkv, Wu, bfull);
-  split2h<<<128 * D_ / 4 / 256, 256, 0, stream>>>(Wu,
+  prep_a<<<16469, 256, 0, stream>>>(x, Wqkv, Wo, W1, W2, Wg,
+                                    (unsigned short*)xh, (unsigned short*)xls,
+                                    (unsigned short*)Wqh, (unsigned short*)Wqls,
+                                    Wvh, Wob, W1t, W2t, Wg2, rowtok, dacc);
+  wu_kernel2<<<256, 256, 0, stream>>>(Wqkv, Wg2, bqkv,
       (unsigned short*)(Wqh + (size_t)1024 * D_),
-      (unsigned short*)(Wqls + (size_t)1024 * D_), 128 * D_);
-
-  gemm_split2<<<dim3(9, 64), 256, 0, stream>>>(xh, xls, Wqh, Wqls,
-                                               bfull, qku32, NQKU_, D_);
-  gemm_vf16<<<dim3(4, 64), 256, 0, stream>>>(xh, Wvh, bqkv + 1024, vbuf, D_, D_);
-  ksplit<<<TOK_ * 512 / 4 / 256, 256, 0, stream>>>(qku32, (unsigned short*)kh,
-                                                   (unsigned short*)kls);
-  transpose_u<<<dim3(32, 4), 256, 0, stream>>>(qku32, U2T);
-  xwg_kernel<<<TOK_ / 32, 256, 0, stream>>>(x, bo, Wg, logits);
-  transpose_v<<<dim3(64, 2, 32), 256, 0, stream>>>((const unsigned short*)vbuf,
-                                                   (unsigned short*)vT);
-
+      (unsigned short*)(Wqls + (size_t)1024 * D_), bfull);
+  gemm_qv<<<832, 256, 0, stream>>>(xh, xls, Wqh, Wqls, bfull, qku32,
+                                   Wvh, bqkv + 1024, vbuf);
+  prep_e<<<8576, 256, 0, stream>>>(qku32, (unsigned short*)kh,
+                                   (unsigned short*)kls, U2T, x, bo, Wg,
+                                   logits, (const unsigned short*)vbuf,
+                                   (unsigned short*)vT);
   attn_fused<<<dim3(1024), 256, 0, stream>>>(qku32, kh, kls, vT, U2T,
                                              attnb, part);
-  gemm_mfma<1><<<dim3(4, 64), 256, 0, stream>>>(attnb, Wob, bo, x, o2,
-                                                D_, D_, nullptr, nullptr);
-  reduce_gate<<<TOK_ / 256, 256, 0, stream>>>(logits, part, e1a, e2a, g1a, g2a,
-                                              use2a, dacc);
+  wo_rg<<<288, 256, 0, stream>>>(attnb, Wob, bo, x, o2, logits, part,
+                                 e1a, e2a, g1a, g2a, use2a, dacc);
   scan_kernel<<<B_, 512, 0, stream>>>(e1a, e2a, use2a, posArr, kept_be);
   finalize_meta<<<1, 64, 0, stream>>>(kept_be, ebase, bbase, ecnt, dacc,
                                       out + (size_t)TOK_ * D_);
```

Result: faster. 433.1 us (-8.5%).
